# Kernel optimization log

Hardware: AMD Instinct MI355X
Metric: run time of the kernel (lower is better)

Reference implementation:

```python
import jax, jax.numpy as jnp
import numpy as np

# FTDEA(e_hidden=300, r_hidden=100, t_hidden=100)
N_NODES = 50000
N_EDGES = 250000
N_EDGES_ALL = 500000
N_REL = 300
EH, RH, TH = 300, 100, 100


def _seg_softmax(logits, seg, num):
    # torch_geometric.utils.softmax: segment-wise stable softmax
    m = jax.ops.segment_max(logits, seg, num_segments=num)
    e = jnp.exp(logits - m[seg])
    s = jax.ops.segment_sum(e, seg, num_segments=num)
    return e / s[seg]


def _gcn(x, j, i, n):
    deg = jax.ops.segment_sum(jnp.ones(i.shape[0], x.dtype), i, num_segments=n)
    dinv = jnp.where(deg > 0, 1.0 / jnp.sqrt(jnp.maximum(deg, 1.0)), 0.0)
    norm = dinv[j] * dinv[i]
    return jax.nn.relu(jax.ops.segment_sum(norm[:, None] * x[j], i, num_segments=n))


def setup_inputs():
    key = jax.random.key(0)
    ks = jax.random.split(key, 32)
    f32 = jnp.float32

    def w(k, shape):
        return jax.random.normal(k, shape, f32) / np.float32(np.sqrt(shape[0]))

    inp = {
        "x": jax.random.normal(ks[0], (N_NODES, EH), f32),
        "edge_index": jax.random.randint(ks[1], (2, N_EDGES), 0, N_NODES),
        "rel": jax.random.randint(ks[2], (N_EDGES,), 0, N_REL),
        "edge_index_all": jax.random.randint(ks[3], (2, N_EDGES_ALL), 0, N_NODES),
        "rel_size": jnp.arange(N_EDGES),
        "hw1_w": w(ks[4], (EH, EH)), "hw1_b": jnp.zeros((EH,), f32),
        "hw2_w": w(ks[5], (EH, EH)), "hw2_b": jnp.zeros((EH,), f32),
        "tc1_w": w(ks[6], (EH, TH)), "tc1_b": jnp.zeros((TH,), f32),
        "sr1_w": w(ks[7], (2 * TH, RH)), "sr1_b": jnp.zeros((RH,), f32),
        "a1_w": w(ks[8], (RH,)), "a5_w": w(ks[9], (RH,)),
        "wr_w": w(ks[10], (RH + 2 * TH, EH)), "wr_b": jnp.zeros((EH,), f32),
        "wr1_w": w(ks[11], (RH + 2 * TH, EH)), "wr1_b": jnp.zeros((EH,), f32),
        "wr2_w": w(ks[12], (RH + 2 * TH, EH)), "wr2_b": jnp.zeros((EH,), f32),
        "ah_w": w(ks[13], (EH,)), "ah1_w": w(ks[14], (EH,)), "at_w": w(ks[15], (EH,)),
        "ar1_w": w(ks[16], (EH,)), "ar2_w": w(ks[17], (EH,)), "ar3_w": w(ks[18], (EH,)),
        "ai_w": w(ks[19], (EH,)), "aj_w": w(ks[20], (EH,)),
        "fc_w": w(ks[21], (2 * EH,)), "fc_b": jnp.zeros((1,), f32),
    }
    return inp


def _forward(x, hw1_w, hw1_b, hw2_w, hw2_b, tc1_w, tc1_b, sr1_w, sr1_b, a1_w, a5_w,
             wr_w, wr_b, wr1_w, wr1_b, wr2_w, wr2_b, ah_w, ah1_w, at_w,
             ar1_w, ar2_w, ar3_w, ai_w, aj_w, fc_w, fc_b,
             edge_index, rel, edge_index_all, rel_size):
    N = x.shape[0]
    E = rel.shape[0]
    h, t = edge_index[0], edge_index[1]
    j, i = edge_index_all[0], edge_index_all[1]
    lrelu = jax.nn.leaky_relu  # slope 0.01 == F.leaky_relu default

    def highway(x1, x2, wg, bg):
        gate = jax.nn.sigmoid(x1 @ wg + bg)
        return gate * x2 + (1.0 - gate) * x1

    x = highway(x, _gcn(x, j, i, N), hw1_w, hw1_b)
    x = highway(x, _gcn(x, j, i, N), hw2_w, hw2_b)

    # --- GATt_to_R. NB: FTDEA overwrites gat_e_to_r output with zeros, so
    # x_res1 input is all-zeros and GAT_E_to_R is mathematically dead code.
    # Also r_in_t1 aliases r_in_t in the torch code, so the in-place per-relation
    # mean loop rewrites BOTH -> r_in_t1 = per-relation mean features.
    s = x @ tc1_w + tc1_b                                    # [N, t]
    cnt = jnp.maximum(jax.ops.segment_sum(jnp.ones(E, x.dtype), rel, num_segments=N_REL), 1.0)[:, None]
    mh = jax.ops.segment_sum(s[h], rel, num_segments=N_REL) / cnt
    mt = jax.ops.segment_sum(s[t], rel, num_segments=N_REL) / cnt
    r_in_t1 = jnp.concatenate([mh, mt], axis=1)[rel]         # [E, 2t]
    x_res2 = r_in_t1 @ sr1_w + sr1_b                         # [E, r]
    x_res1 = jnp.zeros((E, RH), x.dtype)                     # zeroed GAT_E_to_R output
    e1 = x_res2 @ a1_w + x_res1 @ a5_w                       # [E]
    alpha = _seg_softmax(lrelu(e1), rel, N_REL)
    x_type = jax.ops.segment_sum(alpha[:, None] * x_res2[rel_size], rel, num_segments=N_REL)  # spmm
    r_f = jnp.concatenate([x_res1 + x_type[rel], r_in_t1], axis=1)   # [E, r+2t]

    # --- GATr_to_e: three attention rounds (head, tail, head) ---
    def r2e(x_e, wr, br, a_node, a_rel, idx):
        e_r = r_f @ wr + br                                  # [E, e]
        logits = x_e[idx] @ a_node + e_r @ a_rel             # [E]
        a = _seg_softmax(lrelu(logits), idx, N)
        agg = jax.nn.relu(jax.ops.segment_sum(a[:, None] * e_r[rel_size], idx, num_segments=N))
        return x_e + agg

    x = r2e(x, wr_w, wr_b, ah_w, ar1_w, h)
    x = r2e(x, wr1_w, wr1_b, at_w, ar2_w, t)
    x = r2e(x, wr2_w, wr2_b, ah1_w, ar3_w, h)

    # --- GAT_act over edge_index_all ---
    logits = (x @ ai_w)[i] + (x @ aj_w)[j]
    a = _seg_softmax(lrelu(logits), i, N)
    g = jax.nn.relu(jax.ops.segment_sum(a[:, None] * x[j], i, num_segments=N))

    return jnp.concatenate([x, g], axis=1) @ fc_w + fc_b[0]  # [N]


def reference(x, edge_index, rel, edge_index_all, rel_size, hw1_w, hw1_b, hw2_w, hw2_b,
              tc1_w, tc1_b, sr1_w, sr1_b, a1_w, a5_w, wr_w, wr_b, wr1_w, wr1_b,
              wr2_w, wr2_b, ah_w, ah1_w, at_w, ar1_w, ar2_w, ar3_w, ai_w, aj_w, fc_w, fc_b):
    return _forward(x, hw1_w, hw1_b, hw2_w, hw2_b, tc1_w, tc1_b, sr1_w, sr1_b, a1_w, a5_w,
                    wr_w, wr_b, wr1_w, wr1_b, wr2_w, wr2_b, ah_w, ah1_w, at_w,
                    ar1_w, ar2_w, ar3_w, ai_w, aj_w, fc_w, fc_b,
                    edge_index, rel, edge_index_all, rel_size)
```

## Files before the change

kernel.cpp:

```cpp
#include <hip/hip_runtime.h>
#include <hip/hip_bf16.h>

typedef __hip_bfloat16 bf16;
typedef __attribute__((ext_vector_type(8))) short bf16x8_t;
typedef __attribute__((ext_vector_type(4))) float f32x4_t;

__device__ __forceinline__ float b2f(bf16 v){ return __bfloat162float(v); }
__device__ __forceinline__ bf16 f2b(float v){ return __float2bfloat16(v); }
__device__ __forceinline__ short tobits(float v){ bf16 b = f2b(v); return *(short*)&b; }
__device__ __forceinline__ float us2f(ushort u){ return __uint_as_float(((unsigned)u)<<16); }
__device__ __forceinline__ ushort f2us(float v){ bf16 b = f2b(v); return *(ushort*)&b; }

#define NN 50000
#define NE 250000
#define NEA 500000
#define NR 300
#define EHD 300
#define THD 100
#define RHD 100
#define RCH 8
#define NBN 98
#define NBR 75

__device__ __forceinline__ int clampi(int v, int n){ return ((unsigned)v < (unsigned)n) ? v : 0; }

__device__ __forceinline__ float wred_sum(float p){
    #pragma unroll
    for(int m=32;m>=1;m>>=1) p += __shfl_xor(p, m);
    return p;
}
__device__ __forceinline__ float wred_max(float p){
    #pragma unroll
    for(int m=32;m>=1;m>>=1) p = fmaxf(p, __shfl_xor(p, m));
    return p;
}

__global__ void k_zero_f32(float* __restrict__ p, int n){
    int i = blockIdx.x*256 + threadIdx.x;
    if(i < n) p[i] = 0.f;
}

__global__ void k_prep(const float4* __restrict__ xin4, ushort* __restrict__ xFu,
                       const float* __restrict__ hw1w, const float* __restrict__ hw2w,
                       const float* __restrict__ tc1w,
                       short* __restrict__ Wt1, short* __restrict__ Wt2, short* __restrict__ Wtc,
                       int* __restrict__ bcnt){
    int i = blockIdx.x*256 + threadIdx.x;
    if(i < 512) bcnt[i] = 0;
    const int N4 = NN*EHD/4;
    if(i < N4){
        float4 v = xin4[i];
        ushort4 o;
        o.x = (ushort)tobits(v.x); o.y = (ushort)tobits(v.y);
        o.z = (ushort)tobits(v.z); o.w = (ushort)tobits(v.w);
        *(ushort4*)(xFu + 4*(size_t)i) = o;
    }
    const int S1 = EHD*EHD, S2 = 2*EHD*EHD, S3 = 2*EHD*EHD + EHD*THD;
    if(i < S1){
        int n = i/EHD, k = i - n*EHD;
        Wt1[i] = tobits(hw1w[(size_t)k*EHD + n]);
    } else if(i < S2){
        int ii = i - S1; int n = ii/EHD, k = ii - n*EHD;
        Wt2[ii] = tobits(hw2w[(size_t)k*EHD + n]);
    } else if(i < S3){
        int ii = i - S2; int n = ii/EHD, k = ii - n*EHD;
        Wtc[ii] = tobits(tc1w[(size_t)k*THD + n]);
    }
}

__global__ __launch_bounds__(256) void k_bincnt(const int* __restrict__ ji, const int* __restrict__ ht,
                         const int* __restrict__ rel, int* __restrict__ bcnt){
    int s = blockIdx.y;
    int n_s = (s == 0) ? NEA : NE;
    int base_e = blockIdx.x*2048;
    if(base_e >= n_s) return;
    int shift = (s < 3) ? 9 : 2;
    int tid = threadIdx.x;
    __shared__ int h[128];
    if(tid < 128) h[tid] = 0;
    __syncthreads();
    #pragma unroll
    for(int u=0;u<8;u++){
        int e = base_e + u*256 + tid;
        if(e < n_s){
            int key;
            if(s == 0) key = clampi(ji[NEA + e], NN);
            else if(s == 1) key = clampi(ht[e], NN);
            else if(s == 2) key = clampi(ht[NE + e], NN);
            else key = clampi(rel[e], NR);
            atomicAdd(&h[key >> shift], 1);
        }
    }
    __syncthreads();
    if(tid < 128 && h[tid] > 0) atomicAdd(&bcnt[s*128 + tid], h[tid]);
}

__global__ void k_bscan(const int* __restrict__ bcnt, int* __restrict__ gbase, int* __restrict__ gcur){
    __shared__ int lds[512];
    int tid = threadIdx.x;
    int v = bcnt[tid];
    lds[tid] = v; __syncthreads();
    for(int st=1; st<128; st<<=1){
        int add = ((tid & 127) >= st) ? lds[tid-st] : 0;
        __syncthreads();
        lds[tid] += add;
        __syncthreads();
    }
    int s = tid >> 7, b = tid & 127;
    int excl = lds[tid] - v;
    gbase[s*129 + b] = excl;
    gcur[s*128 + b] = excl;
    if(b == 127) gbase[s*129 + 128] = lds[tid];
}

__global__ __launch_bounds__(256) void k_bin(const int* __restrict__ ji, const int* __restrict__ ht,
                      const int* __restrict__ rel, int* __restrict__ gcur,
                      int2* __restrict__ t0, int2* __restrict__ t1,
                      int2* __restrict__ t2, int2* __restrict__ t3){
    int s = blockIdx.y;
    int n_s = (s == 0) ? NEA : NE;
    int base_e = blockIdx.x*2048;
    if(base_e >= n_s) return;
    int shift = (s < 3) ? 9 : 2;
    int tid = threadIdx.x;
    __shared__ int cnt[128], lof[128], base[128];
    __shared__ int2 buf[2048];
    if(tid < 128) cnt[tid] = 0;
    __syncthreads();
    int kk[8], pp[8], bb[8], ss[8];
    #pragma unroll
    for(int u=0;u<8;u++){
        int e = base_e + u*256 + tid;
        bb[u] = -1;
        if(e < n_s){
            int key, pay;
            if(s == 0){ key = clampi(ji[NEA + e], NN); pay = clampi(ji[e], NN); }
            else if(s == 1){ key = clampi(ht[e], NN); pay = clampi(rel[e], NR); }
            else if(s == 2){ key = clampi(ht[NE + e], NN); pay = clampi(rel[e], NR); }
            else { key = clampi(rel[e], NR); pay = e; }
            int b = key >> shift;
            kk[u] = key; pp[u] = pay; bb[u] = b;
            ss[u] = atomicAdd(&cnt[b], 1);
        }
    }
    __syncthreads();
    if(tid == 0){
        int run = 0;
        for(int b=0;b<128;b++){ lof[b] = run; run += cnt[b]; }
    }
    __syncthreads();
    #pragma unroll
    for(int u=0;u<8;u++){
        if(bb[u] >= 0){
            int pos = lof[bb[u]] + ss[u];
            buf[pos] = make_int2(kk[u], pp[u]);
        }
    }
    __syncthreads();
    if(tid < 128 && cnt[tid] > 0) base[tid] = atomicAdd(&gcur[s*128 + tid], cnt[tid]);
    __syncthreads();
    int2* tmp = (s==0) ? t0 : (s==1) ? t1 : (s==2) ? t2 : t3;
    int total = lof[127] + cnt[127];
    for(int idx=tid; idx<total; idx+=256){
        int2 kp = buf[idx];
        int b = kp.x >> shift;
        tmp[base[b] + (idx - lof[b])] = kp;
    }
}

__global__ __launch_bounds__(256) void k_place(const int* __restrict__ gbase,
                        const int2* __restrict__ t0, const int2* __restrict__ t1,
                        const int2* __restrict__ t2, const int2* __restrict__ t3,
                        int* __restrict__ off_all, int* __restrict__ off_h,
                        int* __restrict__ off_t, int* __restrict__ off_r,
                        int* __restrict__ adj_all, int* __restrict__ adj_h,
                        int* __restrict__ adj_t, int* __restrict__ adj_r,
                        float* __restrict__ dinv){
    int s = blockIdx.y, b = blockIdx.x;
    int NB = (s < 3) ? NBN : NBR;
    if(b >= NB) return;
    int W = (s < 3) ? 512 : 4;
    int len = (s < 3) ? NN : NR;
    const int2* tmp = (s==0) ? t0 : (s==1) ? t1 : (s==2) ? t2 : t3;
    int* off = (s==0) ? off_all : (s==1) ? off_h : (s==2) ? off_t : off_r;
    int* adj = (s==0) ? adj_all : (s==1) ? adj_h : (s==2) ? adj_t : adj_r;
    int node0 = b*W;
    int node1 = node0 + W; if(node1 > len) node1 = len;
    int nloc = node1 - node0;
    int wstart = gbase[s*129 + b], wend = gbase[s*129 + b + 1];
    __shared__ int hist[512];
    __shared__ int cur[512];
    __shared__ int sb[256];
    int tid = threadIdx.x;
    for(int k=tid; k<nloc; k+=256) hist[k] = 0;
    __syncthreads();
    for(int idx = wstart + tid; idx < wend; idx += 256){
        int local = tmp[idx].x - node0;
        if((unsigned)local < (unsigned)nloc) atomicAdd(&hist[local], 1);
    }
    __syncthreads();
    int v0 = (2*tid   < nloc) ? hist[2*tid]   : 0;
    int v1 = (2*tid+1 < nloc) ? hist[2*tid+1] : 0;
    int ps = v0 + v1;
    sb[tid] = ps; __syncthreads();
    for(int st=1; st<256; st<<=1){
        int add = (tid >= st) ? sb[tid-st] : 0;
        __syncthreads();
        sb[tid] += add;
        __syncthreads();
    }
    int excl = sb[tid] - ps;
    if(2*tid < nloc){
        int o = wstart + excl;
        off[node0 + 2*tid] = o;
        cur[2*tid] = o;
        if(s == 0) dinv[node0 + 2*tid] = v0 > 0 ? rsqrtf((float)v0) : 0.f;
    }
    if(2*tid+1 < nloc){
        int o = wstart + excl + v0;
        off[node0 + 2*tid+1] = o;
        cur[2*tid+1] = o;
        if(s == 0) dinv[node0 + 2*tid+1] = v1 > 0 ? rsqrtf((float)v1) : 0.f;
    }
    if(b == NB-1 && tid == 0) off[len] = gbase[s*129 + 128];
    __syncthreads();
    for(int idx = wstart + tid; idx < wend; idx += 256){
        int2 kp = tmp[idx];
        int local = kp.x - node0;
        if((unsigned)local < (unsigned)nloc){
            int slot = atomicAdd(&cur[local], 1);
            adj[slot] = kp.y;
        }
    }
}

__global__ void k_gcn(const bf16* __restrict__ xs, bf16* __restrict__ xd,
                      const int* __restrict__ off, const int* __restrict__ adjj,
                      const float* __restrict__ dinv){
    int wid = threadIdx.x >> 6, lane = threadIdx.x & 63;
    int n = blockIdx.x*4 + wid;
    if(n >= NN) return;
    float di = dinv[n];
    int s0 = off[n], s1 = off[n+1], cnt = s1 - s0;
    bool tail = lane < 11;
    float a0=0,a1=0,a2=0,a3=0, t0=0,t1=0,t2=0,t3=0;
    if(cnt > 0 && cnt <= 64){
        int jl = (lane < cnt) ? clampi(adjj[s0+lane], NN) : 0;
        float dl = (lane < cnt) ? dinv[jl] : 0.f;
        int it = 0;
        for(; it+4 <= cnt; it += 4){
            int j0=__shfl(jl,it), j1=__shfl(jl,it+1), j2=__shfl(jl,it+2), j3=__shfl(jl,it+3);
            float n0=di*__shfl(dl,it), n1=di*__shfl(dl,it+1), n2=di*__shfl(dl,it+2), n3=di*__shfl(dl,it+3);
            const ushort4* r0 = (const ushort4*)(xs + (size_t)j0*EHD);
            const ushort4* r1 = (const ushort4*)(xs + (size_t)j1*EHD);
            const ushort4* r2 = (const ushort4*)(xs + (size_t)j2*EHD);
            const ushort4* r3 = (const ushort4*)(xs + (size_t)j3*EHD);
            ushort4 v0=r0[lane], v1=r1[lane], v2=r2[lane], v3=r3[lane];
            a0 += n0*us2f(v0.x)+n1*us2f(v1.x)+n2*us2f(v2.x)+n3*us2f(v3.x);
            a1 += n0*us2f(v0.y)+n1*us2f(v1.y)+n2*us2f(v2.y)+n3*us2f(v3.y);
            a2 += n0*us2f(v0.z)+n1*us2f(v1.z)+n2*us2f(v2.z)+n3*us2f(v3.z);
            a3 += n0*us2f(v0.w)+n1*us2f(v1.w)+n2*us2f(v2.w)+n3*us2f(v3.w);
            if(tail){
                ushort4 u0=r0[64+lane], u1=r1[64+lane], u2=r2[64+lane], u3=r3[64+lane];
                t0 += n0*us2f(u0.x)+n1*us2f(u1.x)+n2*us2f(u2.x)+n3*us2f(u3.x);
                t1 += n0*us2f(u0.y)+n1*us2f(u1.y)+n2*us2f(u2.y)+n3*us2f(u3.y);
                t2 += n0*us2f(u0.z)+n1*us2f(u1.z)+n2*us2f(u2.z)+n3*us2f(u3.z);
                t3 += n0*us2f(u0.w)+n1*us2f(u1.w)+n2*us2f(u2.w)+n3*us2f(u3.w);
            }
        }
        for(; it < cnt; it++){
            int j0 = __shfl(jl, it);
            float n0 = di*__shfl(dl, it);
            const ushort4* r0 = (const ushort4*)(xs + (size_t)j0*EHD);
            ushort4 v0 = r0[lane];
            a0 += n0*us2f(v0.x); a1 += n0*us2f(v0.y); a2 += n0*us2f(v0.z); a3 += n0*us2f(v0.w);
            if(tail){
                ushort4 u0 = r0[64+lane];
                t0 += n0*us2f(u0.x); t1 += n0*us2f(u0.y); t2 += n0*us2f(u0.z); t3 += n0*us2f(u0.w);
            }
        }
    } else if(cnt > 64){
        for(int it=s0; it<s1; it++){
            int j = clampi(adjj[it], NN);
            float nr = di * dinv[j];
            const ushort4* row = (const ushort4*)(xs + (size_t)j*EHD);
            ushort4 v = row[lane];
            a0 += nr*us2f(v.x); a1 += nr*us2f(v.y); a2 += nr*us2f(v.z); a3 += nr*us2f(v.w);
            if(tail){
                ushort4 u = row[64+lane];
                t0 += nr*us2f(u.x); t1 += nr*us2f(u.y); t2 += nr*us2f(u.z); t3 += nr*us2f(u.w);
            }
        }
    }
    ushort4* o = (ushort4*)(xd + (size_t)n*EHD);
    ushort4 w0; w0.x=f2us(fmaxf(a0,0.f)); w0.y=f2us(fmaxf(a1,0.f)); w0.z=f2us(fmaxf(a2,0.f)); w0.w=f2us(fmaxf(a3,0.f));
    o[lane] = w0;
    if(tail){
        ushort4 w1; w1.x=f2us(fmaxf(t0,0.f)); w1.y=f2us(fmaxf(t1,0.f)); w1.z=f2us(fmaxf(t2,0.f)); w1.w=f2us(fmaxf(t3,0.f));
        o[64+lane] = w1;
    }
}

template<int MODE>
__global__ __launch_bounds__(256) void k_gemm_mfma(const bf16* __restrict__ X,
                       const short* __restrict__ Wt, const float* __restrict__ bias,
                       bf16* __restrict__ out, const bf16* __restrict__ Xprev,
                       int M, int K, int Ncols){
    __shared__ short As[64][40];
    __shared__ short Bs[64][40];
    int tid = threadIdx.x;
    int bm = blockIdx.x*64, bn = blockIdx.y*64;
    int wid = tid>>6, lane = tid&63;
    int wm = (wid&1)*32, wn = (wid>>1)*32;
    int lm = lane&15, lq = lane>>4;
    f32x4_t acc00={0,0,0,0}, acc01={0,0,0,0}, acc10={0,0,0,0}, acc11={0,0,0,0};
    int mrow = tid>>2, kc = (tid&3)*8;
    union U8 { bf16x8_t v; uint2 u[2]; short s[8]; };
    for(int k0=0; k0<K; k0+=32){
        int gk0 = k0 + kc;
        {
            int gm = bm + mrow;
            U8 a;
            if(gm < M && gk0 + 8 <= K){
                const uint2* src = (const uint2*)(X + (size_t)gm*K + gk0);
                a.u[0] = src[0]; a.u[1] = src[1];
            } else {
                #pragma unroll
                for(int j=0;j<8;j++){
                    int gk = gk0 + j;
                    a.s[j] = (gm < M && gk < K) ? (short)*(const short*)(X + (size_t)gm*K + gk) : (short)0;
                }
                if(gm >= M){ a.u[0] = {0,0}; a.u[1] = {0,0}; }
            }
            *(bf16x8_t*)&As[mrow][kc] = a.v;
        }
        {
            int gn = bn + mrow;
            U8 b;
            if(gn < Ncols && gk0 + 8 <= K){
                const uint2* src = (const uint2*)(Wt + (size_t)gn*K + gk0);
                b.u[0] = src[0]; b.u[1] = src[1];
            } else {
                #pragma unroll
                for(int j=0;j<8;j++){
                    int gk = gk0 + j;
                    b.s[j] = (gn < Ncols && gk < K) ? Wt[(size_t)gn*K + gk] : (short)0;
                }
                if(gn >= Ncols){ b.u[0] = {0,0}; b.u[1] = {0,0}; }
            }
            *(bf16x8_t*)&Bs[mrow][kc] = b.v;
        }
        __syncthreads();
        bf16x8_t a0 = *(bf16x8_t*)&As[wm + lm][lq*8];
        bf16x8_t a1 = *(bf16x8_t*)&As[wm + 16 + lm][lq*8];
        bf16x8_t b0 = *(bf16x8_t*)&Bs[wn + lm][lq*8];
        bf16x8_t b1 = *(bf16x8_t*)&Bs[wn + 16 + lm][lq*8];
        acc00 = __builtin_amdgcn_mfma_f32_16x16x32_bf16(a0, b0, acc00, 0, 0, 0);
        acc01 = __builtin_amdgcn_mfma_f32_16x16x32_bf16(a0, b1, acc01, 0, 0, 0);
        acc10 = __builtin_amdgcn_mfma_f32_16x16x32_bf16(a1, b0, acc10, 0, 0, 0);
        acc11 = __builtin_amdgcn_mfma_f32_16x16x32_bf16(a1, b1, acc11, 0, 0, 0);
        __syncthreads();
    }
    #pragma unroll
    for(int tm=0;tm<2;tm++){
        #pragma unroll
        for(int tn=0;tn<2;tn++){
            f32x4_t a = tm==0 ? (tn==0 ? acc00 : acc01) : (tn==0 ? acc10 : acc11);
            int gn = bn + wn + tn*16 + lm;
            if(gn >= Ncols) continue;
            float bi = bias[gn];
            #pragma unroll
            for(int r=0;r<4;r++){
                int gm = bm + wm + tm*16 + lq*4 + r;
                if(gm >= M) continue;
                float t = a[r] + bi;
                size_t p = (size_t)gm*Ncols + gn;
                if(MODE == 0){
                    out[p] = f2b(t);
                } else {
                    float g = 1.f/(1.f + expf(-t));
                    out[p] = f2b(g*b2f(out[p]) + (1.f - g)*b2f(Xprev[p]));
                }
            }
        }
    }
}

__global__ void k_relsum2(const bf16* __restrict__ s, const int* __restrict__ ht,
                          const int* __restrict__ off_r, const int* __restrict__ adj_r,
                          float* __restrict__ RF){
    int r = blockIdx.x, c = blockIdx.y, d = threadIdx.x;
    int s0 = off_r[r], s1 = off_r[r+1];
    int cnt = s1 - s0;
    if(cnt <= 0) return;
    int per = (cnt + RCH - 1)/RCH;
    int lo = s0 + c*per, hi = lo + per; if(hi > s1) hi = s1;
    if(lo >= hi) return;
    if(d >= THD) return;
    float ah = 0.f, at2 = 0.f;
    for(int it=lo; it<hi; it++){
        int e = clampi(adj_r[it], NE);
        int hh = clampi(ht[e], NN), tt = clampi(ht[NE + e], NN);
        ah  += b2f(s[(size_t)hh*THD + d]);
        at2 += b2f(s[(size_t)tt*THD + d]);
    }
    atomicAdd(&RF[(size_t)r*EHD + THD   + d], ah);
    atomicAdd(&RF[(size_t)r*EHD + 2*THD + d], at2);
}

__global__ void k_relfin(const float* __restrict__ sr1w, const float* __restrict__ sr1b,
                         const int* __restrict__ off_r, float* __restrict__ RF){
    int r = blockIdx.x, d = threadIdx.x;
    int cnt = off_r[r+1] - off_r[r];
    float inv = 1.f/(float)(cnt > 1 ? cnt : 1);
    if(d < THD){
        RF[(size_t)r*EHD + THD   + d] *= inv;
        RF[(size_t)r*EHD + 2*THD + d] *= inv;
    }
    __syncthreads();
    if(d < RHD){
        float v = 0.f;
        if(cnt > 0){
            v = sr1b[d];
            for(int k2=0; k2<2*THD; k2++) v += RF[(size_t)r*EHD + THD + k2] * sr1w[k2*RHD + d];
        }
        RF[(size_t)r*EHD + d] = v;
    }
}

__global__ void k_reler(const float* __restrict__ RF,
                        const float* w0, const float* b0, const float* w1, const float* b1,
                        const float* w2, const float* b2,
                        const float* ar1, const float* ar2, const float* ar3,
                        float* __restrict__ ER, float* __restrict__ cvec){
    int r = blockIdx.x, kk = blockIdx.y;
    const float* w = kk==0 ? w0 : (kk==1 ? w1 : w2);
    const float* b = kk==0 ? b0 : (kk==1 ? b1 : b2);
    const float* a = kk==0 ? ar1 : (kk==1 ? ar2 : ar3);
    int tid = threadIdx.x;
    float pd = 0.f;
    for(int o = tid; o < EHD; o += 256){
        float v = b[o];
        for(int d=0; d<EHD; d++) v += RF[(size_t)r*EHD + d] * w[(size_t)d*EHD + o];
        ER[((size_t)kk*NR + r)*EHD + o] = v;
        pd += v * a[o];
    }
    __shared__ float red[4];
    pd = wred_sum(pd);
    if((tid & 63) == 0) red[tid>>6] = pd;
    __syncthreads();
    if(tid == 0) cvec[kk*NR + r] = red[0]+red[1]+red[2]+red[3];
}

__device__ __forceinline__ void r2e_round(float* xv, bool tail, int lane, int s0, int s1,
        const int* __restrict__ adjrel, const float* __restrict__ ERk,
        const float* __restrict__ ck, const float* __restrict__ anode){
    const float4* an4 = (const float4*)anode;
    float4 am = an4[lane];
    float p = xv[0]*am.x + xv[1]*am.y + xv[2]*am.z + xv[3]*am.w;
    if(tail){
        float4 at = an4[64+lane];
        p += xv[4]*at.x + xv[5]*at.y + xv[6]*at.z + xv[7]*at.w;
    }
    p = wred_sum(p);
    int cnt = s1 - s0;
    if(cnt <= 0) return;
    float a0=0,a1=0,a2=0,a3=0, t0=0,t1=0,t2=0,t3=0;
    if(cnt <= 64){
        int rl = (lane < cnt) ? clampi(adjrel[s0+lane], NR) : 0;
        float lg = p + ck[rl];
        lg = lg > 0 ? lg : 0.01f*lg;
        float mx = wred_max((lane < cnt) ? lg : -1e30f);
        float ex = (lane < cnt) ? expf(lg - mx) : 0.f;
        float ss = wred_sum(ex);
        float al = ex/ss;
        int it = 0;
        for(; it+2 <= cnt; it += 2){
            int r0i = __shfl(rl, it), r1i = __shfl(rl, it+1);
            float q0 = __shfl(al, it), q1 = __shfl(al, it+1);
            const float4* e0p = (const float4*)(ERk + (size_t)r0i*EHD);
            const float4* e1p = (const float4*)(ERk + (size_t)r1i*EHD);
            float4 e0 = e0p[lane], e1 = e1p[lane];
            a0 += q0*e0.x + q1*e1.x; a1 += q0*e0.y + q1*e1.y;
            a2 += q0*e0.z + q1*e1.z; a3 += q0*e0.w + q1*e1.w;
            if(tail){
                float4 f0 = e0p[64+lane], f1 = e1p[64+lane];
                t0 += q0*f0.x + q1*f1.x; t1 += q0*f0.y + q1*f1.y;
                t2 += q0*f0.z + q1*f1.z; t3 += q0*f0.w + q1*f1.w;
            }
        }
        if(it < cnt){
            int r0i = __shfl(rl, it);
            float q0 = __shfl(al, it);
            const float4* e0p = (const float4*)(ERk + (size_t)r0i*EHD);
            float4 e0 = e0p[lane];
            a0 += q0*e0.x; a1 += q0*e0.y; a2 += q0*e0.z; a3 += q0*e0.w;
            if(tail){
                float4 f0 = e0p[64+lane];
                t0 += q0*f0.x; t1 += q0*f0.y; t2 += q0*f0.z; t3 += q0*f0.w;
            }
        }
    } else {
        float mx = -1e30f;
        for(int it=s0; it<s1; it++){
            float lg = p + ck[clampi(adjrel[it], NR)];
            lg = lg > 0 ? lg : 0.01f*lg;
            mx = fmaxf(mx, lg);
        }
        float ss = 0;
        for(int it=s0; it<s1; it++){
            float lg = p + ck[clampi(adjrel[it], NR)];
            lg = lg > 0 ? lg : 0.01f*lg;
            ss += expf(lg - mx);
        }
        for(int it=s0; it<s1; it++){
            int r = clampi(adjrel[it], NR);
            float lg = p + ck[r];
            lg = lg > 0 ? lg : 0.01f*lg;
            float a = expf(lg - mx)/ss;
            const float4* er4 = (const float4*)(ERk + (size_t)r*EHD);
            float4 e0 = er4[lane];
            a0 += a*e0.x; a1 += a*e0.y; a2 += a*e0.z; a3 += a*e0.w;
            if(tail){
                float4 e1 = er4[64+lane];
                t0 += a*e1.x; t1 += a*e1.y; t2 += a*e1.z; t3 += a*e1.w;
            }
        }
    }
    xv[0] += fmaxf(a0,0.f); xv[1] += fmaxf(a1,0.f); xv[2] += fmaxf(a2,0.f); xv[3] += fmaxf(a3,0.f);
    if(tail){
        xv[4] += fmaxf(t0,0.f); xv[5] += fmaxf(t1,0.f); xv[6] += fmaxf(t2,0.f); xv[7] += fmaxf(t3,0.f);
    }
}

__global__ void k_r2e3(bf16* __restrict__ x,
                       const int* __restrict__ off_h, const int* __restrict__ adj_h,
                       const int* __restrict__ off_t, const int* __restrict__ adj_t,
                       const float* __restrict__ ER, const float* __restrict__ cvec,
                       const float* __restrict__ ahw, const float* __restrict__ atw,
                       const float* __restrict__ ah1w, const float* __restrict__ ajw,
                       float* __restrict__ ajv){
    int wid = threadIdx.x >> 6, lane = threadIdx.x & 63;
    int n = blockIdx.x*4 + wid;
    if(n >= NN) return;
    bool tail = lane < 11;
    ushort4* xr4 = (ushort4*)(x + (size_t)n*EHD);
    float xv[8];
    {
        ushort4 v = xr4[lane];
        xv[0]=us2f(v.x); xv[1]=us2f(v.y); xv[2]=us2f(v.z); xv[3]=us2f(v.w);
        if(tail){
            ushort4 u = xr4[64+lane];
            xv[4]=us2f(u.x); xv[5]=us2f(u.y); xv[6]=us2f(u.z); xv[7]=us2f(u.w);
        } else { xv[4]=0; xv[5]=0; xv[6]=0; xv[7]=0; }
    }
    int h0 = off_h[n], h1 = off_h[n+1];
    int t0_ = off_t[n], t1_ = off_t[n+1];
    r2e_round(xv, tail, lane, h0, h1, adj_h, ER,                    cvec,      ahw);
    r2e_round(xv, tail, lane, t0_, t1_, adj_t, ER + (size_t)NR*EHD, cvec+NR,   atw);
    r2e_round(xv, tail, lane, h0, h1, adj_h, ER + (size_t)2*NR*EHD, cvec+2*NR, ah1w);
    {
        const float4* aj4 = (const float4*)ajw;
        float4 am = aj4[lane];
        float p = xv[0]*am.x + xv[1]*am.y + xv[2]*am.z + xv[3]*am.w;
        if(tail){
            float4 at = aj4[64+lane];
            p += xv[4]*at.x + xv[5]*at.y + xv[6]*at.z + xv[7]*at.w;
        }
        p = wred_sum(p);
        if(lane == 0) ajv[n] = p;
    }
    ushort4 w0; w0.x=f2us(xv[0]); w0.y=f2us(xv[1]); w0.z=f2us(xv[2]); w0.w=f2us(xv[3]);
    xr4[lane] = w0;
    if(tail){
        ushort4 w1; w1.x=f2us(xv[4]); w1.y=f2us(xv[5]); w1.z=f2us(xv[6]); w1.w=f2us(xv[7]);
        xr4[64+lane] = w1;
    }
}

__global__ void k_final(const bf16* __restrict__ x, const float* __restrict__ ajv,
                        const int* __restrict__ off, const int* __restrict__ adjj,
                        const float* __restrict__ aiw, const float* __restrict__ fcw,
                        const float* __restrict__ fcb, float* __restrict__ out){
    int wid = threadIdx.x >> 6, lane = threadIdx.x & 63;
    int n = blockIdx.x*4 + wid;
    if(n >= NN) return;
    bool tail = lane < 11;
    const ushort4* xr4 = (const ushort4*)(x + (size_t)n*EHD);
    const float4* ai4 = (const float4*)aiw;
    ushort4 xv = xr4[lane];
    ushort4 xt = tail ? xr4[64+lane] : ushort4{0,0,0,0};
    float4 am = ai4[lane];
    float4 at = tail ? ai4[64+lane] : float4{0,0,0,0};
    float p = us2f(xv.x)*am.x + us2f(xv.y)*am.y + us2f(xv.z)*am.z + us2f(xv.w)*am.w;
    if(tail) p += us2f(xt.x)*at.x + us2f(xt.y)*at.y + us2f(xt.z)*at.z + us2f(xt.w)*at.w;
    p = wred_sum(p);
    int s0 = off[n], s1 = off[n+1], cnt = s1 - s0;
    float a0=0,a1=0,a2=0,a3=0, t0=0,t1=0,t2=0,t3=0;
    if(cnt > 0 && cnt <= 64){
        int jl = (lane < cnt) ? clampi(adjj[s0+lane], NN) : 0;
        float av = (lane < cnt) ? ajv[jl] : 0.f;
        float lg = p + av;
        lg = lg > 0 ? lg : 0.01f*lg;
        float mx = wred_max((lane < cnt) ? lg : -1e30f);
        float ex = (lane < cnt) ? expf(lg - mx) : 0.f;
        float ss = wred_sum(ex);
        float al = ex/ss;
        int it = 0;
        for(; it+4 <= cnt; it += 4){
            int j0=__shfl(jl,it), j1=__shfl(jl,it+1), j2=__shfl(jl,it+2), j3=__shfl(jl,it+3);
            float q0=__shfl(al,it), q1=__shfl(al,it+1), q2=__shfl(al,it+2), q3=__shfl(al,it+3);
            const ushort4* r0 = (const ushort4*)(x + (size_t)j0*EHD);
            const ushort4* r1 = (const ushort4*)(x + (size_t)j1*EHD);
            const ushort4* r2 = (const ushort4*)(x + (size_t)j2*EHD);
            const ushort4* r3 = (const ushort4*)(x + (size_t)j3*EHD);
            ushort4 v0=r0[lane], v1=r1[lane], v2=r2[lane], v3=r3[lane];
            a0 += q0*us2f(v0.x)+q1*us2f(v1.x)+q2*us2f(v2.x)+q3*us2f(v3.x);
            a1 += q0*us2f(v0.y)+q1*us2f(v1.y)+q2*us2f(v2.y)+q3*us2f(v3.y);
            a2 += q0*us2f(v0.z)+q1*us2f(v1.z)+q2*us2f(v2.z)+q3*us2f(v3.z);
            a3 += q0*us2f(v0.w)+q1*us2f(v1.w)+q2*us2f(v2.w)+q3*us2f(v3.w);
            if(tail){
                ushort4 u0=r0[64+lane], u1=r1[64+lane], u2=r2[64+lane], u3=r3[64+lane];
                t0 += q0*us2f(u0.x)+q1*us2f(u1.x)+q2*us2f(u2.x)+q3*us2f(u3.x);
                t1 += q0*us2f(u0.y)+q1*us2f(u1.y)+q2*us2f(u2.y)+q3*us2f(u3.y);
                t2 += q0*us2f(u0.z)+q1*us2f(u1.z)+q2*us2f(u2.z)+q3*us2f(u3.z);
                t3 += q0*us2f(u0.w)+q1*us2f(u1.w)+q2*us2f(u2.w)+q3*us2f(u3.w);
            }
        }
        for(; it < cnt; it++){
            int j0 = __shfl(jl, it);
            float q0 = __shfl(al, it);
            const ushort4* r0 = (const ushort4*)(x + (size_t)j0*EHD);
            ushort4 v0 = r0[lane];
            a0 += q0*us2f(v0.x); a1 += q0*us2f(v0.y); a2 += q0*us2f(v0.z); a3 += q0*us2f(v0.w);
            if(tail){
                ushort4 u0 = r0[64+lane];
                t0 += q0*us2f(u0.x); t1 += q0*us2f(u0.y); t2 += q0*us2f(u0.z); t3 += q0*us2f(u0.w);
            }
        }
    } else if(cnt > 64){
        float mx = -1e30f;
        for(int it=s0; it<s1; it++){
            float lg = p + ajv[clampi(adjj[it], NN)];
            lg = lg > 0 ? lg : 0.01f*lg;
            mx = fmaxf(mx, lg);
        }
        float ss = 0;
        for(int it=s0; it<s1; it++){
            float lg = p + ajv[clampi(adjj[it], NN)];
            lg = lg > 0 ? lg : 0.01f*lg;
            ss += expf(lg - mx);
        }
        for(int it=s0; it<s1; it++){
            int j = clampi(adjj[it], NN);
            float lg = p + ajv[j];
            lg = lg > 0 ? lg : 0.01f*lg;
            float a = expf(lg - mx)/ss;
            const ushort4* row = (const ushort4*)(x + (size_t)j*EHD);
            ushort4 v = row[lane];
            a0 += a*us2f(v.x); a1 += a*us2f(v.y); a2 += a*us2f(v.z); a3 += a*us2f(v.w);
            if(tail){
                ushort4 u = row[64+lane];
                t0 += a*us2f(u.x); t1 += a*us2f(u.y); t2 += a*us2f(u.z); t3 += a*us2f(u.w);
            }
        }
    }
    const float4* f4 = (const float4*)fcw;
    float4 f0 = f4[lane];
    float4 g0 = f4[75 + lane];
    float part = us2f(xv.x)*f0.x + us2f(xv.y)*f0.y + us2f(xv.z)*f0.z + us2f(xv.w)*f0.w
               + fmaxf(a0,0.f)*g0.x + fmaxf(a1,0.f)*g0.y + fmaxf(a2,0.f)*g0.z + fmaxf(a3,0.f)*g0.w;
    if(tail){
        float4 f1 = f4[64 + lane];
        float4 g1 = f4[139 + lane];
        part += us2f(xt.x)*f1.x + us2f(xt.y)*f1.y + us2f(xt.z)*f1.z + us2f(xt.w)*f1.w
              + fmaxf(t0,0.f)*g1.x + fmaxf(t1,0.f)*g1.y + fmaxf(t2,0.f)*g1.z + fmaxf(t3,0.f)*g1.w;
    }
    part = wred_sum(part);
    if(lane == 0) out[n] = part + fcb[0];
}

extern "C" void kernel_launch(void* const* d_in, const int* in_sizes, int n_in,
                              void* d_out, int out_size, void* d_ws, size_t ws_size,
                              hipStream_t stream){
    const float* x_in = (const float*)d_in[0];
    const int*  ht   = (const int*)d_in[1];
    const int*  rel  = (const int*)d_in[2];
    const int*  ji   = (const int*)d_in[3];
    const float* hw1w=(const float*)d_in[5];  const float* hw1b=(const float*)d_in[6];
    const float* hw2w=(const float*)d_in[7];  const float* hw2b=(const float*)d_in[8];
    const float* tc1w=(const float*)d_in[9];  const float* tc1b=(const float*)d_in[10];
    const float* sr1w=(const float*)d_in[11]; const float* sr1b=(const float*)d_in[12];
    const float* wrw =(const float*)d_in[15]; const float* wrb =(const float*)d_in[16];
    const float* wr1w=(const float*)d_in[17]; const float* wr1b=(const float*)d_in[18];
    const float* wr2w=(const float*)d_in[19]; const float* wr2b=(const float*)d_in[20];
    const float* ahw =(const float*)d_in[21]; const float* ah1w=(const float*)d_in[22];
    const float* atw =(const float*)d_in[23];
    const float* ar1 =(const float*)d_in[24]; const float* ar2 =(const float*)d_in[25];
    const float* ar3 =(const float*)d_in[26];
    const float* aiw =(const float*)d_in[27]; const float* ajw =(const float*)d_in[28];
    const float* fcw =(const float*)d_in[29]; const float* fcb =(const float*)d_in[30];
    float* out = (float*)d_out;

    char* w = (char*)d_ws;
    auto alloc = [&](size_t bytes)->char*{ char* p = w; w += (bytes + 255)/256*256; return p; };
    bf16* xF = (bf16*)alloc((size_t)NN*EHD*2);
    bf16* B  = (bf16*)alloc((size_t)NN*EHD*2);
    char* Bc = (char*)B;
    int2* tmp_all = (int2*)(Bc);
    int2* tmp_h   = (int2*)(Bc + 4u*1024*1024);
    int2* tmp_t   = (int2*)(Bc + 8u*1024*1024);
    int2* tmp_r   = (int2*)(Bc + 12u*1024*1024);
    bf16*  sbuf = (bf16*)(Bc);
    float* RF   = (float*)(Bc + 11u*1024*1024);
    float* ER   = (float*)(Bc + 12u*1024*1024);
    float* cvec = (float*)(Bc + 14u*1024*1024);
    float* ajv  = (float*)(Bc + 15u*1024*1024);
    short* Wt1 = (short*)alloc((size_t)EHD*EHD*2);
    short* Wt2 = (short*)alloc((size_t)EHD*EHD*2);
    short* Wtc = (short*)alloc((size_t)EHD*THD*2);
    float* dinv = (float*)alloc((size_t)NN*4);
    int* off_all=(int*)alloc((NN+1)*4);
    int* adj_all=(int*)alloc((size_t)NEA*4);
    int* off_h  =(int*)alloc((NN+1)*4);
    int* adj_h  =(int*)alloc((size_t)NE*4);
    int* off_t  =(int*)alloc((NN+1)*4);
    int* adj_t  =(int*)alloc((size_t)NE*4);
    int* off_r  =(int*)alloc((NR+1)*4);
    int* adj_r  =(int*)alloc((size_t)NE*4);
    int* bcnt   =(int*)alloc(512*4);
    int* gbase  =(int*)alloc(4*129*4);
    int* gcur   =(int*)alloc(4*128*4);

    const int NPREP = NN*EHD/4;
    k_prep<<<dim3((NPREP+255)/256), dim3(256), 0, stream>>>((const float4*)x_in, (ushort*)xF,
                                                            hw1w, hw2w, tc1w, Wt1, Wt2, Wtc, bcnt);
    k_bincnt<<<dim3((NEA+2047)/2048, 4), dim3(256), 0, stream>>>(ji, ht, rel, bcnt);
    k_bscan<<<dim3(1), dim3(512), 0, stream>>>(bcnt, gbase, gcur);
    k_bin<<<dim3((NEA+2047)/2048, 4), dim3(256), 0, stream>>>(ji, ht, rel, gcur,
                                                              tmp_all, tmp_h, tmp_t, tmp_r);
    k_place<<<dim3(NBN, 4), dim3(256), 0, stream>>>(gbase, tmp_all, tmp_h, tmp_t, tmp_r,
                                                    off_all, off_h, off_t, off_r,
                                                    adj_all, adj_h, adj_t, adj_r, dinv);

    const int nb4 = (NN+3)/4;
    const dim3 gg((NN+63)/64, (EHD+63)/64);
    k_gcn<<<dim3(nb4), dim3(256), 0, stream>>>(xF, B, off_all, adj_all, dinv);
    k_gemm_mfma<1><<<gg, dim3(256), 0, stream>>>(xF, Wt1, hw1b, B, xF, NN, EHD, EHD);
    k_gcn<<<dim3(nb4), dim3(256), 0, stream>>>(B, xF, off_all, adj_all, dinv);
    k_gemm_mfma<1><<<gg, dim3(256), 0, stream>>>(B, Wt2, hw2b, xF, B, NN, EHD, EHD);
    k_gemm_mfma<0><<<dim3((NN+63)/64, (THD+63)/64), dim3(256), 0, stream>>>(xF, Wtc, tc1b, sbuf, xF, NN, EHD, THD);
    k_zero_f32<<<dim3((NR*EHD+255)/256), dim3(256), 0, stream>>>(RF, NR*EHD);
    k_relsum2<<<dim3(NR, RCH), dim3(128), 0, stream>>>(sbuf, ht, off_r, adj_r, RF);
    k_relfin<<<dim3(NR), dim3(128), 0, stream>>>(sr1w, sr1b, off_r, RF);
    k_reler<<<dim3(NR, 3), dim3(256), 0, stream>>>(RF, wrw, wrb, wr1w, wr1b, wr2w, wr2b,
                                                   ar1, ar2, ar3, ER, cvec);
    k_r2e3<<<dim3(nb4), dim3(256), 0, stream>>>(xF, off_h, adj_h, off_t, adj_t, ER, cvec,
                                                ahw, atw, ah1w, ajw, ajv);
    k_final<<<dim3(nb4), dim3(256), 0, stream>>>(xF, ajv, off_all, adj_all, aiw, fcw, fcb, out);
}
```

Baseline: 733.8 us.

## Pad feature rows to 320 and use 16-byte gathers across kernels

Node feature buffers and weight matrices are padded from 300 to 320 columns (zero-filled), so each gather row is 40 aligned 16-byte vectors handled by 40 lanes instead of ushort4 plus a tail. The GEMM loses its K/N boundary checks, relation sums write per-chunk partials instead of atomics (dropping the zero kernel), wave reductions use DPP, and exp/div use fast intrinsics. Padding adds about 7% memory traffic and leaves 24 of 64 lanes idle in the gather kernels. The fast exp/rcp paths slightly change numerics.

Result: faster. 632.7 us (-13.8%).

```diff
diff --git a/kernel.cpp b/kernel.cpp
--- a/kernel.cpp
+++ b/kernel.cpp
@@ -3,6 +3,7 @@
 
 typedef __hip_bfloat16 bf16;
 typedef __attribute__((ext_vector_type(8))) short bf16x8_t;
+typedef __attribute__((ext_vector_type(8))) unsigned short u16x8;
 typedef __attribute__((ext_vector_type(4))) float f32x4_t;
 
 __device__ __forceinline__ float b2f(bf16 v){ return __bfloat162float(v); }
@@ -18,53 +19,87 @@
 #define EHD 300
 #define THD 100
 #define RHD 100
+#define XP 320
+#define ERP 320
 #define RCH 8
 #define NBN 98
 #define NBR 75
 
 __device__ __forceinline__ int clampi(int v, int n){ return ((unsigned)v < (unsigned)n) ? v : 0; }
 
-__device__ __forceinline__ float wred_sum(float p){
-    #pragma unroll
-    for(int m=32;m>=1;m>>=1) p += __shfl_xor(p, m);
-    return p;
-}
-__device__ __forceinline__ float wred_max(float p){
-    #pragma unroll
-    for(int m=32;m>=1;m>>=1) p = fmaxf(p, __shfl_xor(p, m));
-    return p;
-}
-
-__global__ void k_zero_f32(float* __restrict__ p, int n){
-    int i = blockIdx.x*256 + threadIdx.x;
-    if(i < n) p[i] = 0.f;
-}
-
-__global__ void k_prep(const float4* __restrict__ xin4, ushort* __restrict__ xFu,
+__device__ __forceinline__ float dpp_sum(float x){
+    int v;
+    v = __builtin_amdgcn_update_dpp(0, __float_as_int(x), 0x111, 0xf, 0xf, true); x += __int_as_float(v);
+    v = __builtin_amdgcn_update_dpp(0, __float_as_int(x), 0x112, 0xf, 0xf, true); x += __int_as_float(v);
+    v = __builtin_amdgcn_update_dpp(0, __float_as_int(x), 0x114, 0xf, 0xf, true); x += __int_as_float(v);
+    v = __builtin_amdgcn_update_dpp(0, __float_as_int(x), 0x118, 0xf, 0xf, true); x += __int_as_float(v);
+    v = __builtin_amdgcn_update_dpp(0, __float_as_int(x), 0x142, 0xf, 0xf, true); x += __int_as_float(v);
+    v = __builtin_amdgcn_update_dpp(0, __float_as_int(x), 0x143, 0xf, 0xf, true); x += __int_as_float(v);
+    return __int_as_float(__builtin_amdgcn_readlane(__float_as_int(x), 63));
+}
+__device__ __forceinline__ float dpp_max(float x){
+    int v;
+    v = __builtin_amdgcn_update_dpp(__float_as_int(x), __float_as_int(x), 0x111, 0xf, 0xf, false); x = fmaxf(x, __int_as_float(v));
+    v = __builtin_amdgcn_update_dpp(__float_as_int(x), __float_as_int(x), 0x112, 0xf, 0xf, false); x = fmaxf(x, __int_as_float(v));
+    v = __builtin_amdgcn_update_dpp(__float_as_int(x), __float_as_int(x), 0x114, 0xf, 0xf, false); x = fmaxf(x, __int_as_float(v));
+    v = __builtin_amdgcn_update_dpp(__float_as_int(x), __float_as_int(x), 0x118, 0xf, 0xf, false); x = fmaxf(x, __int_as_float(v));
+    v = __builtin_amdgcn_update_dpp(__float_as_int(x), __float_as_int(x), 0x142, 0xf, 0xf, false); x = fmaxf(x, __int_as_float(v));
+    v = __builtin_amdgcn_update_dpp(__float_as_int(x), __float_as_int(x), 0x143, 0xf, 0xf, false); x = fmaxf(x, __int_as_float(v));
+    return __int_as_float(__builtin_amdgcn_readlane(__float_as_int(x), 63));
+}
+
+__global__ void k_prep(const float* __restrict__ xin, ushort* __restrict__ xFu,
                        const float* __restrict__ hw1w, const float* __restrict__ hw2w,
                        const float* __restrict__ tc1w,
                        short* __restrict__ Wt1, short* __restrict__ Wt2, short* __restrict__ Wtc,
-                       int* __restrict__ bcnt){
+                       const float* __restrict__ ahw, const float* __restrict__ atw,
+                       const float* __restrict__ ah1w, const float* __restrict__ ajw,
+                       const float* __restrict__ aiw, const float* __restrict__ fcw,
+                       float* __restrict__ apad, int* __restrict__ bcnt){
     int i = blockIdx.x*256 + threadIdx.x;
     if(i < 512) bcnt[i] = 0;
-    const int N4 = NN*EHD/4;
-    if(i < N4){
-        float4 v = xin4[i];
-        ushort4 o;
-        o.x = (ushort)tobits(v.x); o.y = (ushort)tobits(v.y);
-        o.z = (ushort)tobits(v.z); o.w = (ushort)tobits(v.w);
-        *(ushort4*)(xFu + 4*(size_t)i) = o;
-    }
-    const int S1 = EHD*EHD, S2 = 2*EHD*EHD, S3 = 2*EHD*EHD + EHD*THD;
-    if(i < S1){
-        int n = i/EHD, k = i - n*EHD;
-        Wt1[i] = tobits(hw1w[(size_t)k*EHD + n]);
+    const int NC = NN*40;
+    const int S1 = NC + 320*320;
+    const int S2 = S1 + 320*320;
+    const int S3 = S2 + 128*320;
+    const int S4 = S3 + 7*XP;
+    if(i < NC){
+        int nrow = i/40, c8 = i - nrow*40, c = c8*8;
+        ushort o[8];
+        if(c + 8 <= EHD){
+            const float4* src = (const float4*)(xin + (size_t)nrow*EHD + c);
+            float4 v0 = src[0], v1 = src[1];
+            o[0]=f2us(v0.x); o[1]=f2us(v0.y); o[2]=f2us(v0.z); o[3]=f2us(v0.w);
+            o[4]=f2us(v1.x); o[5]=f2us(v1.y); o[6]=f2us(v1.z); o[7]=f2us(v1.w);
+        } else {
+            #pragma unroll
+            for(int k=0;k<8;k++){
+                int cc = c + k;
+                o[k] = (cc < EHD) ? f2us(xin[(size_t)nrow*EHD + cc]) : (ushort)0;
+            }
+        }
+        u16x8 w;
+        #pragma unroll
+        for(int k=0;k<8;k++) w[k] = o[k];
+        *(u16x8*)(xFu + (size_t)nrow*XP + c) = w;
+    } else if(i < S1){
+        int ii = i - NC; int n = ii/320, k = ii - n*320;
+        Wt1[ii] = (n < EHD && k < EHD) ? tobits(hw1w[(size_t)k*EHD + n]) : (short)0;
     } else if(i < S2){
-        int ii = i - S1; int n = ii/EHD, k = ii - n*EHD;
-        Wt2[ii] = tobits(hw2w[(size_t)k*EHD + n]);
+        int ii = i - S1; int n = ii/320, k = ii - n*320;
+        Wt2[ii] = (n < EHD && k < EHD) ? tobits(hw2w[(size_t)k*EHD + n]) : (short)0;
     } else if(i < S3){
-        int ii = i - S2; int n = ii/EHD, k = ii - n*EHD;
-        Wtc[ii] = tobits(tc1w[(size_t)k*THD + n]);
+        int ii = i - S2; int n = ii/320, k = ii - n*320;
+        Wtc[ii] = (n < THD && k < EHD) ? tobits(tc1w[(size_t)k*THD + n]) : (short)0;
+    } else if(i < S4){
+        int ii = i - S3; int v = ii/XP, c = ii - v*XP;
+        float val = 0.f;
+        if(c < EHD){
+            const float* src = (v==0)?ahw:(v==1)?atw:(v==2)?ah1w:(v==3)?ajw:(v==4)?aiw:
+                               (v==5)? fcw : (fcw + EHD);
+            val = src[c];
+        }
+        apad[ii] = val;
     }
 }
 
@@ -242,8 +277,8 @@
     if(n >= NN) return;
     float di = dinv[n];
     int s0 = off[n], s1 = off[n+1], cnt = s1 - s0;
-    bool tail = lane < 11;
-    float a0=0,a1=0,a2=0,a3=0, t0=0,t1=0,t2=0,t3=0;
+    bool act = lane < 40;
+    float c0=0,c1=0,c2=0,c3=0,c4=0,c5=0,c6=0,c7=0;
     if(cnt > 0 && cnt <= 64){
         int jl = (lane < cnt) ? clampi(adjj[s0+lane], NN) : 0;
         float dl = (lane < cnt) ? dinv[jl] : 0.f;
@@ -251,53 +286,46 @@
         for(; it+4 <= cnt; it += 4){
             int j0=__shfl(jl,it), j1=__shfl(jl,it+1), j2=__shfl(jl,it+2), j3=__shfl(jl,it+3);
             float n0=di*__shfl(dl,it), n1=di*__shfl(dl,it+1), n2=di*__shfl(dl,it+2), n3=di*__shfl(dl,it+3);
-            const ushort4* r0 = (const ushort4*)(xs + (size_t)j0*EHD);
-            const ushort4* r1 = (const ushort4*)(xs + (size_t)j1*EHD);
-            const ushort4* r2 = (const ushort4*)(xs + (size_t)j2*EHD);
-            const ushort4* r3 = (const ushort4*)(xs + (size_t)j3*EHD);
-            ushort4 v0=r0[lane], v1=r1[lane], v2=r2[lane], v3=r3[lane];
-            a0 += n0*us2f(v0.x)+n1*us2f(v1.x)+n2*us2f(v2.x)+n3*us2f(v3.x);
-            a1 += n0*us2f(v0.y)+n1*us2f(v1.y)+n2*us2f(v2.y)+n3*us2f(v3.y);
-            a2 += n0*us2f(v0.z)+n1*us2f(v1.z)+n2*us2f(v2.z)+n3*us2f(v3.z);
-            a3 += n0*us2f(v0.w)+n1*us2f(v1.w)+n2*us2f(v2.w)+n3*us2f(v3.w);
-            if(tail){
-                ushort4 u0=r0[64+lane], u1=r1[64+lane], u2=r2[64+lane], u3=r3[64+lane];
-                t0 += n0*us2f(u0.x)+n1*us2f(u1.x)+n2*us2f(u2.x)+n3*us2f(u3.x);
-                t1 += n0*us2f(u0.y)+n1*us2f(u1.y)+n2*us2f(u2.y)+n3*us2f(u3.y);
-                t2 += n0*us2f(u0.z)+n1*us2f(u1.z)+n2*us2f(u2.z)+n3*us2f(u3.z);
-                t3 += n0*us2f(u0.w)+n1*us2f(u1.w)+n2*us2f(u2.w)+n3*us2f(u3.w);
+            if(act){
+                u16x8 v0 = ((const u16x8*)(xs + (size_t)j0*XP))[lane];
+                u16x8 v1 = ((const u16x8*)(xs + (size_t)j1*XP))[lane];
+                u16x8 v2 = ((const u16x8*)(xs + (size_t)j2*XP))[lane];
+                u16x8 v3 = ((const u16x8*)(xs + (size_t)j3*XP))[lane];
+                c0 += n0*us2f(v0[0])+n1*us2f(v1[0])+n2*us2f(v2[0])+n3*us2f(v3[0]);
+                c1 += n0*us2f(v0[1])+n1*us2f(v1[1])+n2*us2f(v2[1])+n3*us2f(v3[1]);
+                c2 += n0*us2f(v0[2])+n1*us2f(v1[2])+n2*us2f(v2[2])+n3*us2f(v3[2]);
+                c3 += n0*us2f(v0[3])+n1*us2f(v1[3])+n2*us2f(v2[3])+n3*us2f(v3[3]);
+                c4 += n0*us2f(v0[4])+n1*us2f(v1[4])+n2*us2f(v2[4])+n3*us2f(v3[4]);
+                c5 += n0*us2f(v0[5])+n1*us2f(v1[5])+n2*us2f(v2[5])+n3*us2f(v3[5]);
+                c6 += n0*us2f(v0[6])+n1*us2f(v1[6])+n2*us2f(v2[6])+n3*us2f(v3[6]);
+                c7 += n0*us2f(v0[7])+n1*us2f(v1[7])+n2*us2f(v2[7])+n3*us2f(v3[7]);
             }
         }
         for(; it < cnt; it++){
             int j0 = __shfl(jl, it);
             float n0 = di*__shfl(dl, it);
-            const ushort4* r0 = (const ushort4*)(xs + (size_t)j0*EHD);
-            ushort4 v0 = r0[lane];
-            a0 += n0*us2f(v0.x); a1 += n0*us2f(v0.y); a2 += n0*us2f(v0.z); a3 += n0*us2f(v0.w);
-            if(tail){
-                ushort4 u0 = r0[64+lane];
-                t0 += n0*us2f(u0.x); t1 += n0*us2f(u0.y); t2 += n0*us2f(u0.z); t3 += n0*us2f(u0.w);
+            if(act){
+                u16x8 v0 = ((const u16x8*)(xs + (size_t)j0*XP))[lane];
+                c0 += n0*us2f(v0[0]); c1 += n0*us2f(v0[1]); c2 += n0*us2f(v0[2]); c3 += n0*us2f(v0[3]);
+                c4 += n0*us2f(v0[4]); c5 += n0*us2f(v0[5]); c6 += n0*us2f(v0[6]); c7 += n0*us2f(v0[7]);
             }
         }
     } else if(cnt > 64){
         for(int it=s0; it<s1; it++){
             int j = clampi(adjj[it], NN);
             float nr = di * dinv[j];
-            const ushort4* row = (const ushort4*)(xs + (size_t)j*EHD);
-            ushort4 v = row[lane];
-            a0 += nr*us2f(v.x); a1 += nr*us2f(v.y); a2 += nr*us2f(v.z); a3 += nr*us2f(v.w);
-            if(tail){
-                ushort4 u = row[64+lane];
-                t0 += nr*us2f(u.x); t1 += nr*us2f(u.y); t2 += nr*us2f(u.z); t3 += nr*us2f(u.w);
-            }
-        }
-    }
-    ushort4* o = (ushort4*)(xd + (size_t)n*EHD);
-    ushort4 w0; w0.x=f2us(fmaxf(a0,0.f)); w0.y=f2us(fmaxf(a1,0.f)); w0.z=f2us(fmaxf(a2,0.f)); w0.w=f2us(fmaxf(a3,0.f));
-    o[lane] = w0;
-    if(tail){
-        ushort4 w1; w1.x=f2us(fmaxf(t0,0.f)); w1.y=f2us(fmaxf(t1,0.f)); w1.z=f2us(fmaxf(t2,0.f)); w1.w=f2us(fmaxf(t3,0.f));
-        o[64+lane] = w1;
+            if(act){
+                u16x8 v0 = ((const u16x8*)(xs + (size_t)j*XP))[lane];
+                c0 += nr*us2f(v0[0]); c1 += nr*us2f(v0[1]); c2 += nr*us2f(v0[2]); c3 += nr*us2f(v0[3]);
+                c4 += nr*us2f(v0[4]); c5 += nr*us2f(v0[5]); c6 += nr*us2f(v0[6]); c7 += nr*us2f(v0[7]);
+            }
+        }
+    }
+    if(act){
+        u16x8 w;
+        w[0]=f2us(fmaxf(c0,0.f)); w[1]=f2us(fmaxf(c1,0.f)); w[2]=f2us(fmaxf(c2,0.f)); w[3]=f2us(fmaxf(c3,0.f));
+        w[4]=f2us(fmaxf(c4,0.f)); w[5]=f2us(fmaxf(c5,0.f)); w[6]=f2us(fmaxf(c6,0.f)); w[7]=f2us(fmaxf(c7,0.f));
+        ((u16x8*)(xd + (size_t)n*XP))[lane] = w;
     }
 }
 
@@ -305,7 +333,7 @@
 __global__ __launch_bounds__(256) void k_gemm_mfma(const bf16* __restrict__ X,
                        const short* __restrict__ Wt, const float* __restrict__ bias,
                        bf16* __restrict__ out, const bf16* __restrict__ Xprev,
-                       int M, int K, int Ncols){
+                       int M, int K, int Ncols, int ldOut){
     __shared__ short As[64][40];
     __shared__ short Bs[64][40];
     int tid = threadIdx.x;
@@ -315,39 +343,22 @@
     int lm = lane&15, lq = lane>>4;
     f32x4_t acc00={0,0,0,0}, acc01={0,0,0,0}, acc10={0,0,0,0}, acc11={0,0,0,0};
     int mrow = tid>>2, kc = (tid&3)*8;
-    union U8 { bf16x8_t v; uint2 u[2]; short s[8]; };
+    bool fullM = (bm + 64 <= M);
+    union U8 { bf16x8_t v; uint2 u[2]; };
     for(int k0=0; k0<K; k0+=32){
-        int gk0 = k0 + kc;
         {
             int gm = bm + mrow;
             U8 a;
-            if(gm < M && gk0 + 8 <= K){
-                const uint2* src = (const uint2*)(X + (size_t)gm*K + gk0);
+            if(fullM || gm < M){
+                const uint2* src = (const uint2*)(X + (size_t)gm*K + k0 + kc);
                 a.u[0] = src[0]; a.u[1] = src[1];
-            } else {
-                #pragma unroll
-                for(int j=0;j<8;j++){
-                    int gk = gk0 + j;
-                    a.s[j] = (gm < M && gk < K) ? (short)*(const short*)(X + (size_t)gm*K + gk) : (short)0;
-                }
-                if(gm >= M){ a.u[0] = {0,0}; a.u[1] = {0,0}; }
-            }
+            } else { a.u[0] = {0,0}; a.u[1] = {0,0}; }
             *(bf16x8_t*)&As[mrow][kc] = a.v;
         }
         {
-            int gn = bn + mrow;
             U8 b;
-            if(gn < Ncols && gk0 + 8 <= K){
-                const uint2* src = (const uint2*)(Wt + (size_t)gn*K + gk0);
-                b.u[0] = src[0]; b.u[1] = src[1];
-            } else {
-                #pragma unroll
-                for(int j=0;j<8;j++){
-                    int gk = gk0 + j;
-                    b.s[j] = (gn < Ncols && gk < K) ? Wt[(size_t)gn*K + gk] : (short)0;
-                }
-                if(gn >= Ncols){ b.u[0] = {0,0}; b.u[1] = {0,0}; }
-            }
+            const uint2* src = (const uint2*)(Wt + (size_t)(bn + mrow)*K + k0 + kc);
+            b.u[0] = src[0]; b.u[1] = src[1];
             *(bf16x8_t*)&Bs[mrow][kc] = b.v;
         }
         __syncthreads();
@@ -374,11 +385,11 @@
                 int gm = bm + wm + tm*16 + lq*4 + r;
                 if(gm >= M) continue;
                 float t = a[r] + bi;
-                size_t p = (size_t)gm*Ncols + gn;
+                size_t p = (size_t)gm*ldOut + gn;
                 if(MODE == 0){
                     out[p] = f2b(t);
                 } else {
-                    float g = 1.f/(1.f + expf(-t));
+                    float g = __builtin_amdgcn_rcpf(1.f + __expf(-t));
                     out[p] = f2b(g*b2f(out[p]) + (1.f - g)*b2f(Xprev[p]));
                 }
             }
@@ -388,34 +399,43 @@
 
 __global__ void k_relsum2(const bf16* __restrict__ s, const int* __restrict__ ht,
                           const int* __restrict__ off_r, const int* __restrict__ adj_r,
-                          float* __restrict__ RF){
+                          float* __restrict__ RFpart){
     int r = blockIdx.x, c = blockIdx.y, d = threadIdx.x;
+    if(d >= THD) return;
     int s0 = off_r[r], s1 = off_r[r+1];
     int cnt = s1 - s0;
-    if(cnt <= 0) return;
-    int per = (cnt + RCH - 1)/RCH;
-    int lo = s0 + c*per, hi = lo + per; if(hi > s1) hi = s1;
-    if(lo >= hi) return;
-    if(d >= THD) return;
     float ah = 0.f, at2 = 0.f;
-    for(int it=lo; it<hi; it++){
-        int e = clampi(adj_r[it], NE);
-        int hh = clampi(ht[e], NN), tt = clampi(ht[NE + e], NN);
-        ah  += b2f(s[(size_t)hh*THD + d]);
-        at2 += b2f(s[(size_t)tt*THD + d]);
-    }
-    atomicAdd(&RF[(size_t)r*EHD + THD   + d], ah);
-    atomicAdd(&RF[(size_t)r*EHD + 2*THD + d], at2);
+    if(cnt > 0){
+        int per = (cnt + RCH - 1)/RCH;
+        int lo = s0 + c*per, hi = lo + per; if(hi > s1) hi = s1;
+        for(int it=lo; it<hi; it++){
+            int e = clampi(adj_r[it], NE);
+            int hh = clampi(ht[e], NN), tt = clampi(ht[NE + e], NN);
+            ah  += b2f(s[(size_t)hh*THD + d]);
+            at2 += b2f(s[(size_t)tt*THD + d]);
+        }
+    }
+    size_t base = (size_t)(r*RCH + c)*2*THD;
+    RFpart[base + d] = ah;
+    RFpart[base + THD + d] = at2;
 }
 
 __global__ void k_relfin(const float* __restrict__ sr1w, const float* __restrict__ sr1b,
-                         const int* __restrict__ off_r, float* __restrict__ RF){
+                         const int* __restrict__ off_r, const float* __restrict__ RFpart,
+                         float* __restrict__ RF){
     int r = blockIdx.x, d = threadIdx.x;
     int cnt = off_r[r+1] - off_r[r];
     float inv = 1.f/(float)(cnt > 1 ? cnt : 1);
     if(d < THD){
-        RF[(size_t)r*EHD + THD   + d] *= inv;
-        RF[(size_t)r*EHD + 2*THD + d] *= inv;
+        float a = 0.f, b = 0.f;
+        #pragma unroll
+        for(int c=0;c<RCH;c++){
+            size_t base = (size_t)(r*RCH + c)*2*THD;
+            a += RFpart[base + d];
+            b += RFpart[base + THD + d];
+        }
+        RF[(size_t)r*EHD + THD   + d] = a*inv;
+        RF[(size_t)r*EHD + 2*THD + d] = b*inv;
     }
     __syncthreads();
     if(d < RHD){
@@ -438,66 +458,70 @@
     const float* b = kk==0 ? b0 : (kk==1 ? b1 : b2);
     const float* a = kk==0 ? ar1 : (kk==1 ? ar2 : ar3);
     int tid = threadIdx.x;
+    __shared__ float rfs[EHD];
+    for(int d=tid; d<EHD; d+=256) rfs[d] = RF[(size_t)r*EHD + d];
+    __syncthreads();
     float pd = 0.f;
-    for(int o = tid; o < EHD; o += 256){
-        float v = b[o];
-        for(int d=0; d<EHD; d++) v += RF[(size_t)r*EHD + d] * w[(size_t)d*EHD + o];
-        ER[((size_t)kk*NR + r)*EHD + o] = v;
-        pd += v * a[o];
+    for(int o = tid; o < ERP; o += 256){
+        float v = 0.f;
+        if(o < EHD){
+            v = b[o];
+            for(int d=0; d<EHD; d++) v += rfs[d] * w[(size_t)d*EHD + o];
+            pd += v * a[o];
+        }
+        ER[((size_t)kk*NR + r)*ERP + o] = v;
     }
     __shared__ float red[4];
-    pd = wred_sum(pd);
+    pd = dpp_sum(pd);
     if((tid & 63) == 0) red[tid>>6] = pd;
     __syncthreads();
     if(tid == 0) cvec[kk*NR + r] = red[0]+red[1]+red[2]+red[3];
 }
 
-__device__ __forceinline__ void r2e_round(float* xv, bool tail, int lane, int s0, int s1,
+__device__ __forceinline__ void r2e_round(float* xv, bool act, int lane, int s0, int s1,
+        int rl, float cval,
         const int* __restrict__ adjrel, const float* __restrict__ ERk,
-        const float* __restrict__ ck, const float* __restrict__ anode){
-    const float4* an4 = (const float4*)anode;
-    float4 am = an4[lane];
-    float p = xv[0]*am.x + xv[1]*am.y + xv[2]*am.z + xv[3]*am.w;
-    if(tail){
-        float4 at = an4[64+lane];
-        p += xv[4]*at.x + xv[5]*at.y + xv[6]*at.z + xv[7]*at.w;
-    }
-    p = wred_sum(p);
+        const float* __restrict__ ck, const float* __restrict__ an){
+    float p = 0.f;
+    if(act){
+        const float4* a4 = (const float4*)an;
+        float4 a0 = a4[2*lane], a1 = a4[2*lane+1];
+        p = xv[0]*a0.x + xv[1]*a0.y + xv[2]*a0.z + xv[3]*a0.w
+          + xv[4]*a1.x + xv[5]*a1.y + xv[6]*a1.z + xv[7]*a1.w;
+    }
+    p = dpp_sum(p);
     int cnt = s1 - s0;
     if(cnt <= 0) return;
-    float a0=0,a1=0,a2=0,a3=0, t0=0,t1=0,t2=0,t3=0;
+    float c0=0,c1=0,c2=0,c3=0,c4=0,c5=0,c6=0,c7=0;
     if(cnt <= 64){
-        int rl = (lane < cnt) ? clampi(adjrel[s0+lane], NR) : 0;
-        float lg = p + ck[rl];
+        float lg = p + cval;
         lg = lg > 0 ? lg : 0.01f*lg;
-        float mx = wred_max((lane < cnt) ? lg : -1e30f);
-        float ex = (lane < cnt) ? expf(lg - mx) : 0.f;
-        float ss = wred_sum(ex);
-        float al = ex/ss;
+        float mx = dpp_max((lane < cnt) ? lg : -1e30f);
+        float ex = (lane < cnt) ? __expf(lg - mx) : 0.f;
+        float al = ex * __builtin_amdgcn_rcpf(dpp_sum(ex));
         int it = 0;
         for(; it+2 <= cnt; it += 2){
             int r0i = __shfl(rl, it), r1i = __shfl(rl, it+1);
             float q0 = __shfl(al, it), q1 = __shfl(al, it+1);
-            const float4* e0p = (const float4*)(ERk + (size_t)r0i*EHD);
-            const float4* e1p = (const float4*)(ERk + (size_t)r1i*EHD);
-            float4 e0 = e0p[lane], e1 = e1p[lane];
-            a0 += q0*e0.x + q1*e1.x; a1 += q0*e0.y + q1*e1.y;
-            a2 += q0*e0.z + q1*e1.z; a3 += q0*e0.w + q1*e1.w;
-            if(tail){
-                float4 f0 = e0p[64+lane], f1 = e1p[64+lane];
-                t0 += q0*f0.x + q1*f1.x; t1 += q0*f0.y + q1*f1.y;
-                t2 += q0*f0.z + q1*f1.z; t3 += q0*f0.w + q1*f1.w;
+            if(act){
+                const float4* e0p = (const float4*)(ERk + (size_t)r0i*ERP);
+                const float4* e1p = (const float4*)(ERk + (size_t)r1i*ERP);
+                float4 e0 = e0p[2*lane], e1 = e1p[2*lane];
+                float4 f0 = e0p[2*lane+1], f1 = e1p[2*lane+1];
+                c0 += q0*e0.x + q1*e1.x; c1 += q0*e0.y + q1*e1.y;
+                c2 += q0*e0.z + q1*e1.z; c3 += q0*e0.w + q1*e1.w;
+                c4 += q0*f0.x + q1*f1.x; c5 += q0*f0.y + q1*f1.y;
+                c6 += q0*f0.z + q1*f1.z; c7 += q0*f0.w + q1*f1.w;
             }
         }
         if(it < cnt){
             int r0i = __shfl(rl, it);
             float q0 = __shfl(al, it);
-            const float4* e0p = (const float4*)(ERk + (size_t)r0i*EHD);
-            float4 e0 = e0p[lane];
-            a0 += q0*e0.x; a1 += q0*e0.y; a2 += q0*e0.z; a3 += q0*e0.w;
-            if(tail){
-                float4 f0 = e0p[64+lane];
-                t0 += q0*f0.x; t1 += q0*f0.y; t2 += q0*f0.z; t3 += q0*f0.w;
+            if(act){
+                const float4* e0p = (const float4*)(ERk + (size_t)r0i*ERP);
+                float4 e0 = e0p[2*lane], f0 = e0p[2*lane+1];
+                c0 += q0*e0.x; c1 += q0*e0.y; c2 += q0*e0.z; c3 += q0*e0.w;
+                c4 += q0*f0.x; c5 += q0*f0.y; c6 += q0*f0.z; c7 += q0*f0.w;
             }
         }
     } else {
@@ -507,135 +531,138 @@
             lg = lg > 0 ? lg : 0.01f*lg;
             mx = fmaxf(mx, lg);
         }
-        float ss = 0;
+        float ssum = 0.f;
         for(int it=s0; it<s1; it++){
             float lg = p + ck[clampi(adjrel[it], NR)];
             lg = lg > 0 ? lg : 0.01f*lg;
-            ss += expf(lg - mx);
-        }
+            ssum += __expf(lg - mx);
+        }
+        float rinv = __builtin_amdgcn_rcpf(ssum);
         for(int it=s0; it<s1; it++){
             int r = clampi(adjrel[it], NR);
             float lg = p + ck[r];
             lg = lg > 0 ? lg : 0.01f*lg;
-            float a = expf(lg - mx)/ss;
-            const float4* er4 = (const float4*)(ERk + (size_t)r*EHD);
-            float4 e0 = er4[lane];
-            a0 += a*e0.x; a1 += a*e0.y; a2 += a*e0.z; a3 += a*e0.w;
-            if(tail){
-                float4 e1 = er4[64+lane];
-                t0 += a*e1.x; t1 += a*e1.y; t2 += a*e1.z; t3 += a*e1.w;
-            }
-        }
-    }
-    xv[0] += fmaxf(a0,0.f); xv[1] += fmaxf(a1,0.f); xv[2] += fmaxf(a2,0.f); xv[3] += fmaxf(a3,0.f);
-    if(tail){
-        xv[4] += fmaxf(t0,0.f); xv[5] += fmaxf(t1,0.f); xv[6] += fmaxf(t2,0.f); xv[7] += fmaxf(t3,0.f);
-    }
+            float aw = __expf(lg - mx)*rinv;
+            if(act){
+                const float4* er4 = (const float4*)(ERk + (size_t)r*ERP);
+                float4 e0 = er4[2*lane], f0 = er4[2*lane+1];
+                c0 += aw*e0.x; c1 += aw*e0.y; c2 += aw*e0.z; c3 += aw*e0.w;
+                c4 += aw*f0.x; c5 += aw*f0.y; c6 += aw*f0.z; c7 += aw*f0.w;
+            }
+        }
+    }
+    xv[0] += fmaxf(c0,0.f); xv[1] += fmaxf(c1,0.f); xv[2] += fmaxf(c2,0.f); xv[3] += fmaxf(c3,0.f);
+    xv[4] += fmaxf(c4,0.f); xv[5] += fmaxf(c5,0.f); xv[6] += fmaxf(c6,0.f); xv[7] += fmaxf(c7,0.f);
 }
 
 __global__ void k_r2e3(bf16* __restrict__ x,
                        const int* __restrict__ off_h, const int* __restrict__ adj_h,
                        const int* __restrict__ off_t, const int* __restrict__ adj_t,
                        const float* __restrict__ ER, const float* __restrict__ cvec,
-                       const float* __restrict__ ahw, const float* __restrict__ atw,
-                       const float* __restrict__ ah1w, const float* __restrict__ ajw,
-                       float* __restrict__ ajv){
+                       const float* __restrict__ apad, float* __restrict__ ajv){
     int wid = threadIdx.x >> 6, lane = threadIdx.x & 63;
     int n = blockIdx.x*4 + wid;
     if(n >= NN) return;
-    bool tail = lane < 11;
-    ushort4* xr4 = (ushort4*)(x + (size_t)n*EHD);
+    bool act = lane < 40;
+    u16x8* xr = (u16x8*)(x + (size_t)n*XP);
     float xv[8];
-    {
-        ushort4 v = xr4[lane];
-        xv[0]=us2f(v.x); xv[1]=us2f(v.y); xv[2]=us2f(v.z); xv[3]=us2f(v.w);
-        if(tail){
-            ushort4 u = xr4[64+lane];
-            xv[4]=us2f(u.x); xv[5]=us2f(u.y); xv[6]=us2f(u.z); xv[7]=us2f(u.w);
-        } else { xv[4]=0; xv[5]=0; xv[6]=0; xv[7]=0; }
+    if(act){
+        u16x8 v = xr[lane];
+        #pragma unroll
+        for(int k=0;k<8;k++) xv[k] = us2f(v[k]);
+    } else {
+        #pragma unroll
+        for(int k=0;k<8;k++) xv[k] = 0.f;
     }
     int h0 = off_h[n], h1 = off_h[n+1];
     int t0_ = off_t[n], t1_ = off_t[n+1];
-    r2e_round(xv, tail, lane, h0, h1, adj_h, ER,                    cvec,      ahw);
-    r2e_round(xv, tail, lane, t0_, t1_, adj_t, ER + (size_t)NR*EHD, cvec+NR,   atw);
-    r2e_round(xv, tail, lane, h0, h1, adj_h, ER + (size_t)2*NR*EHD, cvec+2*NR, ah1w);
+    int hcnt = h1 - h0, tcnt = t1_ - t0_;
+    int rlh = (hcnt > 0 && hcnt <= 64 && lane < hcnt) ? clampi(adj_h[h0+lane], NR) : 0;
+    int rlt = (tcnt > 0 && tcnt <= 64 && lane < tcnt) ? clampi(adj_t[t0_+lane], NR) : 0;
+    float ch1 = cvec[rlh], ctv = cvec[NR + rlt], ch3 = cvec[2*NR + rlh];
+    r2e_round(xv, act, lane, h0, h1, rlh, ch1, adj_h, ER,                    cvec,      apad);
+    r2e_round(xv, act, lane, t0_, t1_, rlt, ctv, adj_t, ER + (size_t)NR*ERP, cvec+NR,   apad + XP);
+    r2e_round(xv, act, lane, h0, h1, rlh, ch3, adj_h, ER + (size_t)2*NR*ERP, cvec+2*NR, apad + 2*XP);
     {
-        const float4* aj4 = (const float4*)ajw;
-        float4 am = aj4[lane];
-        float p = xv[0]*am.x + xv[1]*am.y + xv[2]*am.z + xv[3]*am.w;
-        if(tail){
-            float4 at = aj4[64+lane];
-            p += xv[4]*at.x + xv[5]*at.y + xv[6]*at.z + xv[7]*at.w;
-        }
-        p = wred_sum(p);
+        float p = 0.f;
+        if(act){
+            const float4* a4 = (const float4*)(apad + 3*XP);
+            float4 a0 = a4[2*lane], a1 = a4[2*lane+1];
+            p = xv[0]*a0.x + xv[1]*a0.y + xv[2]*a0.z + xv[3]*a0.w
+              + xv[4]*a1.x + xv[5]*a1.y + xv[6]*a1.z + xv[7]*a1.w;
+        }
+        p = dpp_sum(p);
         if(lane == 0) ajv[n] = p;
     }
-    ushort4 w0; w0.x=f2us(xv[0]); w0.y=f2us(xv[1]); w0.z=f2us(xv[2]); w0.w=f2us(xv[3]);
-    xr4[lane] = w0;
-    if(tail){
-        ushort4 w1; w1.x=f2us(xv[4]); w1.y=f2us(xv[5]); w1.z=f2us(xv[6]); w1.w=f2us(xv[7]);
-        xr4[64+lane] = w1;
+    if(act){
+        u16x8 w;
+        #pragma unroll
+        for(int k=0;k<8;k++) w[k] = f2us(xv[k]);
+        xr[lane] = w;
     }
 }
 
 __global__ void k_final(const bf16* __restrict__ x, const float* __restrict__ ajv,
                         const int* __restrict__ off, const int* __restrict__ adjj,
-                        const float* __restrict__ aiw, const float* __restrict__ fcw,
-                        const float* __restrict__ fcb, float* __restrict__ out){
+                        const float* __restrict__ apad, const float* __restrict__ fcb,
+                        float* __restrict__ out){
     int wid = threadIdx.x >> 6, lane = threadIdx.x & 63;
     int n = blockIdx.x*4 + wid;
     if(n >= NN) return;
-    bool tail = lane < 11;
-    const ushort4* xr4 = (const ushort4*)(x + (size_t)n*EHD);
-    const float4* ai4 = (const float4*)aiw;
-    ushort4 xv = xr4[lane];
-    ushort4 xt = tail ? xr4[64+lane] : ushort4{0,0,0,0};
-    float4 am = ai4[lane];
-    float4 at = tail ? ai4[64+lane] : float4{0,0,0,0};
-    float p = us2f(xv.x)*am.x + us2f(xv.y)*am.y + us2f(xv.z)*am.z + us2f(xv.w)*am.w;
-    if(tail) p += us2f(xt.x)*at.x + us2f(xt.y)*at.y + us2f(xt.z)*at.z + us2f(xt.w)*at.w;
-    p = wred_sum(p);
+    bool act = lane < 40;
+    float xv[8];
+    if(act){
+        u16x8 v = ((const u16x8*)(x + (size_t)n*XP))[lane];
+        #pragma unroll
+        for(int k=0;k<8;k++) xv[k] = us2f(v[k]);
+    } else {
+        #pragma unroll
+        for(int k=0;k<8;k++) xv[k] = 0.f;
+    }
+    float p = 0.f;
+    if(act){
+        const float4* a4 = (const float4*)(apad + 4*XP);
+        float4 a0 = a4[2*lane], a1 = a4[2*lane+1];
+        p = xv[0]*a0.x + xv[1]*a0.y + xv[2]*a0.z + xv[3]*a0.w
+          + xv[4]*a1.x + xv[5]*a1.y + xv[6]*a1.z + xv[7]*a1.w;
+    }
+    p = dpp_sum(p);
     int s0 = off[n], s1 = off[n+1], cnt = s1 - s0;
-    float a0=0,a1=0,a2=0,a3=0, t0=0,t1=0,t2=0,t3=0;
+    float c0=0,c1=0,c2=0,c3=0,c4=0,c5=0,c6=0,c7=0;
     if(cnt > 0 && cnt <= 64){
         int jl = (lane < cnt) ? clampi(adjj[s0+lane], NN) : 0;
         float av = (lane < cnt) ? ajv[jl] : 0.f;
         float lg = p + av;
         lg = lg > 0 ? lg : 0.01f*lg;
-        float mx = wred_max((lane < cnt) ? lg : -1e30f);
-        float ex = (lane < cnt) ? expf(lg - mx) : 0.f;
-        float ss = wred_sum(ex);
-        float al = ex/ss;
+        float mx = dpp_max((lane < cnt) ? lg : -1e30f);
+        float ex = (lane < cnt) ? __expf(lg - mx) : 0.f;
+        float al = ex * __builtin_amdgcn_rcpf(dpp_sum(ex));
         int it = 0;
         for(; it+4 <= cnt; it += 4){
             int j0=__shfl(jl,it), j1=__shfl(jl,it+1), j2=__shfl(jl,it+2), j3=__shfl(jl,it+3);
             float q0=__shfl(al,it), q1=__shfl(al,it+1), q2=__shfl(al,it+2), q3=__shfl(al,it+3);
-            const ushort4* r0 = (const ushort4*)(x + (size_t)j0*EHD);
-            const ushort4* r1 = (const ushort4*)(x + (size_t)j1*EHD);
-            const ushort4* r2 = (const ushort4*)(x + (size_t)j2*EHD);
-            const ushort4* r3 = (const ushort4*)(x + (size_t)j3*EHD);
-            ushort4 v0=r0[lane], v1=r1[lane], v2=r2[lane], v3=r3[lane];
-            a0 += q0*us2f(v0.x)+q1*us2f(v1.x)+q2*us2f(v2.x)+q3*us2f(v3.x);
-            a1 += q0*us2f(v0.y)+q1*us2f(v1.y)+q2*us2f(v2.y)+q3*us2f(v3.y);
-            a2 += q0*us2f(v0.z)+q1*us2f(v1.z)+q2*us2f(v2.z)+q3*us2f(v3.z);
-            a3 += q0*us2f(v0.w)+q1*us2f(v1.w)+q2*us2f(v2.w)+q3*us2f(v3.w);
-            if(tail){
-                ushort4 u0=r0[64+lane], u1=r1[64+lane], u2=r2[64+lane], u3=r3[64+lane];
-                t0 += q0*us2f(u0.x)+q1*us2f(u1.x)+q2*us2f(u2.x)+q3*us2f(u3.x);
-                t1 += q0*us2f(u0.y)+q1*us2f(u1.y)+q2*us2f(u2.y)+q3*us2f(u3.y);
-                t2 += q0*us2f(u0.z)+q1*us2f(u1.z)+q2*us2f(u2.z)+q3*us2f(u3.z);
-                t3 += q0*us2f(u0.w)+q1*us2f(u1.w)+q2*us2f(u2.w)+q3*us2f(u3.w);
+            if(act){
+                u16x8 v0 = ((const u16x8*)(x + (size_t)j0*XP))[lane];
+                u16x8 v1 = ((const u16x8*)(x + (size_t)j1*XP))[lane];
+                u16x8 v2 = ((const u16x8*)(x + (size_t)j2*XP))[lane];
+                u16x8 v3 = ((const u16x8*)(x + (size_t)j3*XP))[lane];
+                c0 += q0*us2f(v0[0])+q1*us2f(v1[0])+q2*us2f(v2[0])+q3*us2f(v3[0]);
+                c1 += q0*us2f(v0[1])+q1*us2f(v1[1])+q2*us2f(v2[1])+q3*us2f(v3[1]);
+                c2 += q0*us2f(v0[2])+q1*us2f(v1[2])+q2*us2f(v2[2])+q3*us2f(v3[2]);
+                c3 += q0*us2f(v0[3])+q1*us2f(v1[3])+q2*us2f(v2[3])+q3*us2f(v3[3]);
+                c4 += q0*us2f(v0[4])+q1*us2f(v1[4])+q2*us2f(v2[4])+q3*us2f(v3[4]);
+                c5 += q0*us2f(v0[5])+q1*us2f(v1[5])+q2*us2f(v2[5])+q3*us2f(v3[5]);
+                c6 += q0*us2f(v0[6])+q1*us2f(v1[6])+q2*us2f(v2[6])+q3*us2f(v3[6]);
+                c7 += q0*us2f(v0[7])+q1*us2f(v1[7])+q2*us2f(v2[7])+q3*us2f(v3[7]);
             }
         }
         for(; it < cnt; it++){
             int j0 = __shfl(jl, it);
             float q0 = __shfl(al, it);
-            const ushort4* r0 = (const ushort4*)(x + (size_t)j0*EHD);
-            ushort4 v0 = r0[lane];
-            a0 += q0*us2f(v0.x); a1 += q0*us2f(v0.y); a2 += q0*us2f(v0.z); a3 += q0*us2f(v0.w);
-            if(tail){
-                ushort4 u0 = r0[64+lane];
-                t0 += q0*us2f(u0.x); t1 += q0*us2f(u0.y); t2 += q0*us2f(u0.z); t3 += q0*us2f(u0.w);
+            if(act){
+                u16x8 v0 = ((const u16x8*)(x + (size_t)j0*XP))[lane];
+                c0 += q0*us2f(v0[0]); c1 += q0*us2f(v0[1]); c2 += q0*us2f(v0[2]); c3 += q0*us2f(v0[3]);
+                c4 += q0*us2f(v0[4]); c5 += q0*us2f(v0[5]); c6 += q0*us2f(v0[6]); c7 += q0*us2f(v0[7]);
             }
         }
     } else if(cnt > 64){
@@ -645,38 +672,37 @@
             lg = lg > 0 ? lg : 0.01f*lg;
             mx = fmaxf(mx, lg);
         }
-        float ss = 0;
+        float ssum = 0.f;
         for(int it=s0; it<s1; it++){
             float lg = p + ajv[clampi(adjj[it], NN)];
             lg = lg > 0 ? lg : 0.01f*lg;
-            ss += expf(lg - mx);
-        }
+            ssum += __expf(lg - mx);
+        }
+        float rinv = __builtin_amdgcn_rcpf(ssum);
         for(int it=s0; it<s1; it++){
             int j = clampi(adjj[it], NN);
             float lg = p + ajv[j];
             lg = lg > 0 ? lg : 0.01f*lg;
-            float a = expf(lg - mx)/ss;
-            const ushort4* row = (const ushort4*)(x + (size_t)j*EHD);
-            ushort4 v = row[lane];
-            a0 += a*us2f(v.x); a1 += a*us2f(v.y); a2 += a*us2f(v.z); a3 += a*us2f(v.w);
-            if(tail){
-                ushort4 u = row[64+lane];
-                t0 += a*us2f(u.x); t1 += a*us2f(u.y); t2 += a*us2f(u.z); t3 += a*us2f(u.w);
-            }
-        }
-    }
-    const float4* f4 = (const float4*)fcw;
-    float4 f0 = f4[lane];
-    float4 g0 = f4[75 + lane];
-    float part = us2f(xv.x)*f0.x + us2f(xv.y)*f0.y + us2f(xv.z)*f0.z + us2f(xv.w)*f0.w
-               + fmaxf(a0,0.f)*g0.x + fmaxf(a1,0.f)*g0.y + fmaxf(a2,0.f)*g0.z + fmaxf(a3,0.f)*g0.w;
-    if(tail){
-        float4 f1 = f4[64 + lane];
-        float4 g1 = f4[139 + lane];
-        part += us2f(xt.x)*f1.x + us2f(xt.y)*f1.y + us2f(xt.z)*f1.z + us2f(xt.w)*f1.w
-              + fmaxf(t0,0.f)*g1.x + fmaxf(t1,0.f)*g1.y + fmaxf(t2,0.f)*g1.z + fmaxf(t3,0.f)*g1.w;
-    }
-    part = wred_sum(part);
+            float aw = __expf(lg - mx)*rinv;
+            if(act){
+                u16x8 v0 = ((const u16x8*)(x + (size_t)j*XP))[lane];
+                c0 += aw*us2f(v0[0]); c1 += aw*us2f(v0[1]); c2 += aw*us2f(v0[2]); c3 += aw*us2f(v0[3]);
+                c4 += aw*us2f(v0[4]); c5 += aw*us2f(v0[5]); c6 += aw*us2f(v0[6]); c7 += aw*us2f(v0[7]);
+            }
+        }
+    }
+    float part = 0.f;
+    if(act){
+        const float4* f5 = (const float4*)(apad + 5*XP);
+        const float4* f6 = (const float4*)(apad + 6*XP);
+        float4 u0 = f5[2*lane], u1 = f5[2*lane+1];
+        float4 g0 = f6[2*lane], g1 = f6[2*lane+1];
+        part = xv[0]*u0.x + xv[1]*u0.y + xv[2]*u0.z + xv[3]*u0.w
+             + xv[4]*u1.x + xv[5]*u1.y + xv[6]*u1.z + xv[7]*u1.w
+             + fmaxf(c0,0.f)*g0.x + fmaxf(c1,0.f)*g0.y + fmaxf(c2,0.f)*g0.z + fmaxf(c3,0.f)*g0.w
+             + fmaxf(c4,0.f)*g1.x + fmaxf(c5,0.f)*g1.y + fmaxf(c6,0.f)*g1.z + fmaxf(c7,0.f)*g1.w;
+    }
+    part = dpp_sum(part);
     if(lane == 0) out[n] = part + fcb[0];
 }
 
@@ -704,21 +730,23 @@
 
     char* w = (char*)d_ws;
     auto alloc = [&](size_t bytes)->char*{ char* p = w; w += (bytes + 255)/256*256; return p; };
-    bf16* xF = (bf16*)alloc((size_t)NN*EHD*2);
-    bf16* B  = (bf16*)alloc((size_t)NN*EHD*2);
+    bf16* xF = (bf16*)alloc((size_t)NN*XP*2);
+    bf16* B  = (bf16*)alloc((size_t)NN*XP*2);
     char* Bc = (char*)B;
     int2* tmp_all = (int2*)(Bc);
     int2* tmp_h   = (int2*)(Bc + 4u*1024*1024);
     int2* tmp_t   = (int2*)(Bc + 8u*1024*1024);
     int2* tmp_r   = (int2*)(Bc + 12u*1024*1024);
-    bf16*  sbuf = (bf16*)(Bc);
-    float* RF   = (float*)(Bc + 11u*1024*1024);
-    float* ER   = (float*)(Bc + 12u*1024*1024);
-    float* cvec = (float*)(Bc + 14u*1024*1024);
-    float* ajv  = (float*)(Bc + 15u*1024*1024);
-    short* Wt1 = (short*)alloc((size_t)EHD*EHD*2);
-    short* Wt2 = (short*)alloc((size_t)EHD*EHD*2);
-    short* Wtc = (short*)alloc((size_t)EHD*THD*2);
+    bf16*  sbuf   = (bf16*)(Bc);
+    float* RF     = (float*)(Bc + 10u*1024*1024);
+    float* RFpart = (float*)(Bc + 11u*1024*1024);
+    float* ER     = (float*)(Bc + 13u*1024*1024);
+    float* cvec   = (float*)(Bc + 14u*1024*1024 + 512u*1024);
+    float* ajv    = (float*)(Bc + 15u*1024*1024);
+    short* Wt1 = (short*)alloc((size_t)320*320*2);
+    short* Wt2 = (short*)alloc((size_t)320*320*2);
+    short* Wtc = (short*)alloc((size_t)128*320*2);
+    float* apad = (float*)alloc((size_t)7*XP*4);
     float* dinv = (float*)alloc((size_t)NN*4);
     int* off_all=(int*)alloc((NN+1)*4);
     int* adj_all=(int*)alloc((size_t)NEA*4);
@@ -732,9 +760,11 @@
     int* gbase  =(int*)alloc(4*129*4);
     int* gcur   =(int*)alloc(4*128*4);
 
-    const int NPREP = NN*EHD/4;
-    k_prep<<<dim3((NPREP+255)/256), dim3(256), 0, stream>>>((const float4*)x_in, (ushort*)xF,
-                                                            hw1w, hw2w, tc1w, Wt1, Wt2, Wtc, bcnt);
+    const int PRT = NN*40 + 2*320*320 + 128*320 + 7*XP;
+    k_prep<<<dim3((PRT+255)/256), dim3(256), 0, stream>>>(x_in, (ushort*)xF, hw1w, hw2w, tc1w,
+                                                          Wt1, Wt2, Wtc,
+                                                          ahw, atw, ah1w, ajw, aiw, fcw,
+                                                          apad, bcnt);
     k_bincnt<<<dim3((NEA+2047)/2048, 4), dim3(256), 0, stream>>>(ji, ht, rel, bcnt);
     k_bscan<<<dim3(1), dim3(512), 0, stream>>>(bcnt, gbase, gcur);
     k_bin<<<dim3((NEA+2047)/2048, 4), dim3(256), 0, stream>>>(ji, ht, rel, gcur,
@@ -746,16 +776,15 @@
     const int nb4 = (NN+3)/4;
     const dim3 gg((NN+63)/64, (EHD+63)/64);
     k_gcn<<<dim3(nb4), dim3(256), 0, stream>>>(xF, B, off_all, adj_all, dinv);
-    k_gemm_mfma<1><<<gg, dim3(256), 0, stream>>>(xF, Wt1, hw1b, B, xF, NN, EHD, EHD);
+    k_gemm_mfma<1><<<gg, dim3(256), 0, stream>>>(xF, Wt1, hw1b, B, xF, NN, XP, EHD, XP);
     k_gcn<<<dim3(nb4), dim3(256), 0, stream>>>(B, xF, off_all, adj_all, dinv);
-    k_gemm_mfma<1><<<gg, dim3(256), 0, stream>>>(B, Wt2, hw2b, xF, B, NN, EHD, EHD);
-    k_gemm_mfma<0><<<dim3((NN+63)/64, (THD+63)/64), dim3(256), 0, stream>>>(xF, Wtc, tc1b, sbuf, xF, NN, EHD, THD);
-    k_zero_f32<<<dim3((NR*EHD+255)/256), dim3(256), 0, stream>>>(RF, NR*EHD);
-    k_relsum2<<<dim3(NR, RCH), dim3(128), 0, stream>>>(sbuf, ht, off_r, adj_r, RF);
-    k_relfin<<<dim3(NR), dim3(128), 0, stream>>>(sr1w, sr1b, off_r, RF);
+    k_gemm_mfma<1><<<gg, dim3(256), 0, stream>>>(B, Wt2, hw2b, xF, B, NN, XP, EHD, XP);
+    k_gemm_mfma<0><<<dim3((NN+63)/64, (THD+63)/64), dim3(256), 0, stream>>>(xF, Wtc, tc1b, sbuf, xF, NN, XP, THD, THD);
+    k_relsum2<<<dim3(NR, RCH), dim3(128), 0, stream>>>(sbuf, ht, off_r, adj_r, RFpart);
+    k_relfin<<<dim3(NR), dim3(128), 0, stream>>>(sr1w, sr1b, off_r, RFpart, RF);
     k_reler<<<dim3(NR, 3), dim3(256), 0, stream>>>(RF, wrw, wrb, wr1w, wr1b, wr2w, wr2b,
                                                    ar1, ar2, ar3, ER, cvec);
     k_r2e3<<<dim3(nb4), dim3(256), 0, stream>>>(xF, off_h, adj_h, off_t, adj_t, ER, cvec,
-                                                ahw, atw, ah1w, ajw, ajv);
-    k_final<<<dim3(nb4), dim3(256), 0, stream>>>(xF, ajv, off_all, adj_all, aiw, fcw, fcb, out);
-}
+                                                apad, ajv);
+    k_final<<<dim3(nb4), dim3(256), 0, stream>>>(xF, ajv, off_all, adj_all, apad, fcb, out);
+}
```
